# Kernel tuning notes

Hardware: AMD Instinct MI355X
Metric: run time of the kernel (lower is better)

Reference implementation:

```python
import jax, jax.numpy as jnp
import numpy as np

B, NM, NB, Z, H, K = 1024, 20000, 25000, 64, 256, 20
BETA = 0.1
LOG2PI = float(np.log(2.0 * np.pi))


def _log_normal(x, m, v):
    D = x.shape[-1]
    return (-0.5 * D * LOG2PI
            - 0.5 * jnp.sum(jnp.log(v), axis=-1)
            - 0.5 * jnp.sum((x - m) ** 2 / v, axis=-1))


def _kl_gmm(z, q_m, q_logv, p_m, p_logv):
    log_q = _log_normal(z, q_m, jnp.exp(q_logv))                               # [B]
    lp = _log_normal(z[:, None, :], p_m[None], jnp.exp(p_logv)[None])          # [B,K]
    log_p = jax.scipy.special.logsumexp(lp, axis=1) - jnp.log(float(p_m.shape[0]))
    return jnp.sum(log_q - log_p)


def _dist2(x, y):
    # ||x_i - y_j||_2^2, expanded form (avoids the [R,C,D] broadcast of the torch code)
    x2 = jnp.sum(x * x, axis=1, keepdims=True)
    y2 = jnp.sum(y * y, axis=1, keepdims=True)
    return x2 + y2.T - 2.0 * (x @ y.T)


def _distance_gmm(mu_s, mu_d, lv_s, lv_d):
    return _dist2(mu_s, mu_d) + _dist2(jnp.exp(0.5 * lv_s), jnp.exp(0.5 * lv_d)) + 1e-6


def _cost_mat(cost_s, cost_t, tran):
    f1 = jnp.sum(cost_s ** 2, axis=1, keepdims=True) / cost_s.shape[0]  # [ns,1]
    f2 = jnp.sum(cost_t ** 2, axis=1, keepdims=True) / cost_t.shape[0]  # [nt,1]
    return f1 + f2.T - 2.0 * (cost_s @ tran @ cost_t.T)


def _fgw(mu, z_mu, logvar, z_logvar):
    c_post = _distance_gmm(mu, mu, logvar, logvar)
    c_prior = _distance_gmm(z_mu, z_mu, z_logvar, z_logvar)
    c_pp = _distance_gmm(mu, z_mu, logvar, z_logvar)
    ns, nt = c_post.shape[0], c_prior.shape[0]
    p_s = jnp.ones((ns, 1), c_post.dtype) / ns
    p_t = jnp.ones((nt, 1), c_post.dtype) / nt

    def compute_tran(c_post, c_prior, c_pp):
        def outer(carry, _):
            tran, dual = carry
            cost = BETA * _cost_mat(c_post, c_prior, tran) + (1.0 - BETA) * c_pp
            kernel = jnp.exp(-cost / jnp.max(jnp.abs(cost))) * tran
            b = p_t / (kernel.T @ dual)

            def inner(c2, _):
                dual, b = c2
                dual = p_s / (kernel @ b)
                b = p_t / (kernel.T @ dual)
                return (dual, b), None

            (dual, b), _ = jax.lax.scan(inner, (dual, b), None, length=5)
            tran = (dual @ b.T) * kernel
            return (tran, dual), None

        init = (jnp.ones((ns, nt), c_post.dtype) / (ns * nt),
                jnp.ones((ns, 1), c_post.dtype) / ns)
        (tran, _), _ = jax.lax.scan(outer, init, None, length=10)
        return jnp.where(jnp.any(jnp.isnan(tran)),
                         jnp.ones((ns, nt), tran.dtype) / (ns * nt), tran)

    # torch detaches tran before the final cost, so cut all gradient through the loop
    tran = jax.lax.stop_gradient(compute_tran(c_post, c_prior, c_pp))
    cost = BETA * _cost_mat(c_post, c_prior, tran) + (1.0 - BETA) * c_pp
    return jnp.sum(cost * tran)


def _forward(batch_user_x, batch_user_y, p_mu_a, p_logv_a, p_mu_b, p_logv_b,
             eps_x, eps_y, eps_xr, eps_yr,
             W1a, b1a, W21a, b21a, W22a, b22a, W3a, b3a, W4a, b4a,
             W1b, b1b, W21b, b21b, W22b, b22b, W3b, b3b, W4b, b4b):
    def enc_a(x):
        h = jax.nn.relu(x @ W1a + b1a)
        return h @ W21a + b21a, h @ W22a + b22a

    def dec_a(z):
        return jax.nn.relu(z @ W3a + b3a) @ W4a + b4a

    def enc_b(x):
        h = jax.nn.relu(x @ W1b + b1b)
        return h @ W21b + b21b, h @ W22b + b22b

    def dec_b(z):
        return jax.nn.relu(z @ W3b + b3b) @ W4b + b4b

    # dropout rate = 0.0 -> identity
    mu_a, logvar_a = enc_a(batch_user_x)
    z_x = mu_a + eps_x * jnp.exp(0.5 * logvar_a)
    preds_x = dec_a(z_x)
    mu_b, logvar_b = enc_b(batch_user_y)
    z_y = mu_b + eps_y * jnp.exp(0.5 * logvar_b)
    preds_y = dec_b(z_y)

    gmm_reg_loss_a = _kl_gmm(z_x, mu_a, logvar_a, p_mu_a, p_logv_a)
    gmm_reg_loss_b = _kl_gmm(z_y, mu_b, logvar_b, p_mu_b, p_logv_b)
    align_global_loss = _fgw(mu_b, mu_a, logvar_b, logvar_a)

    preds_x2y = dec_b(z_x)
    preds_y2x = dec_a(z_y)
    m_xr, lv_xr = enc_b(preds_x2y)
    feature_x_r = m_xr + eps_xr * jnp.exp(0.5 * lv_xr)
    m_yr, lv_yr = enc_a(preds_y2x)
    feature_y_r = m_yr + eps_yr * jnp.exp(0.5 * lv_yr)

    cyc_loss_x = jnp.linalg.norm(z_x - feature_x_r)
    cyc_loss_y = jnp.linalg.norm(z_y - feature_y_r)
    return (preds_x, preds_y, preds_x2y, preds_y2x, z_x, z_y,
            gmm_reg_loss_a, gmm_reg_loss_b, feature_x_r, feature_y_r,
            align_global_loss, cyc_loss_x, cyc_loss_y)


def setup_inputs() -> dict:
    key = jax.random.key(0)
    ks = jax.random.split(key, 24)

    def nrm(i, shape, s=1.0):
        return jax.random.normal(ks[i], shape, dtype=jnp.float32) * s

    return {
        "user_1": jax.random.randint(ks[0], (B,), 0, 100000),
        "user_2": jax.random.randint(ks[1], (B,), 0, 100000),
        "batch_user_x": jax.random.uniform(ks[2], (B, NM), dtype=jnp.float32),
        "batch_user_y": jax.random.uniform(ks[3], (B, NB), dtype=jnp.float32),
        "p_mu_a": nrm(4, (K, Z)), "p_logv_a": nrm(5, (K, Z), 0.1),
        "p_mu_b": nrm(6, (K, Z)), "p_logv_b": nrm(7, (K, Z), 0.1),
        "eps_x": nrm(8, (B, Z)), "eps_y": nrm(9, (B, Z)),
        "eps_xr": nrm(10, (B, Z)), "eps_yr": nrm(11, (B, Z)),
        "W1a": nrm(12, (NM, H), 0.02), "b1a": jnp.zeros((H,), jnp.float32),
        "W21a": nrm(13, (H, Z), 0.02), "b21a": jnp.zeros((Z,), jnp.float32),
        "W22a": nrm(14, (H, Z), 0.02), "b22a": jnp.zeros((Z,), jnp.float32),
        "W3a": nrm(15, (Z, H), 0.02), "b3a": jnp.zeros((H,), jnp.float32),
        "W4a": nrm(16, (H, NM), 0.02), "b4a": jnp.zeros((NM,), jnp.float32),
        "W1b": nrm(17, (NB, H), 0.02), "b1b": jnp.zeros((H,), jnp.float32),
        "W21b": nrm(18, (H, Z), 0.02), "b21b": jnp.zeros((Z,), jnp.float32),
        "W22b": nrm(19, (H, Z), 0.02), "b22b": jnp.zeros((Z,), jnp.float32),
        "W3b": nrm(20, (Z, H), 0.02), "b3b": jnp.zeros((H,), jnp.float32),
        "W4b": nrm(21, (H, NB), 0.02), "b4b": jnp.zeros((NB,), jnp.float32),
    }


def reference(user_1, user_2, batch_user_x, batch_user_y, p_mu_a, p_logv_a, p_mu_b, p_logv_b,
              eps_x, eps_y, eps_xr, eps_yr,
              W1a, b1a, W21a, b21a, W22a, b22a, W3a, b3a, W4a, b4a,
              W1b, b1b, W21b, b21b, W22b, b22b, W3b, b3b, W4b, b4b):
    # user_1/user_2 are unused by the torch forward as well
    return _forward(batch_user_x, batch_user_y, p_mu_a, p_logv_a, p_mu_b, p_logv_b,
                    eps_x, eps_y, eps_xr, eps_yr,
                    W1a, b1a, W21a, b21a, W22a, b22a, W3a, b3a, W4a, b4a,
                    W1b, b1b, W21b, b21b, W22b, b22b, W3b, b3b, W4b, b4b)
```

## Files before the change

kernel.cpp:

```cpp
#include <hip/hip_runtime.h>


#define DEVI __device__ __forceinline__

typedef __attribute__((ext_vector_type(4))) float  f32x4;
typedef __attribute__((ext_vector_type(4))) short  s16x4;
typedef __attribute__((ext_vector_type(8))) short  s16x8;
typedef __attribute__((ext_vector_type(8))) __bf16 bf16x8;

#define PS (1.f / 1024.f)
#define UNIF (1.f / (1024.f * 1024.f))

DEVI short f2bf(float f) {
  unsigned u = __float_as_uint(f);
  u += 0x7fffu + ((u >> 16) & 1u);
  return (short)(u >> 16);
}
DEVI float bf2f(unsigned short u) { return __uint_as_float(((unsigned)u) << 16); }

DEVI f32x4 mfma16(bf16x8 a, bf16x8 b, f32x4 c) {
  return __builtin_amdgcn_mfma_f32_16x16x32_bf16(a, b, c, 0, 0, 0);
}

struct GemmArgs {
  const float* Af;
  const unsigned short* Bt;
  float* outF;
  const float* bias;
  float* partials;
  int M, N, K;
  int lda, ldbt, ldc;
  int totSteps, nSplits;
};

enum { EPI_PARTIAL, EPI_BIAS, EPI_COST, EPI_LOSS };

template<int BM, int BN, int WR, int WC, int EPI>
DEVI void gemm_body(const GemmArgs g)
{
  constexpr int BK = 64, BKP = 72;
  constexpr int NT = WR * WC * 64;
  __shared__ short As[BM * BKP];
  __shared__ short Bs[BN * BKP];

  const int m0 = blockIdx.x * BM;
  int n0 = 0, kb0 = 0, kb1 = g.K, split = 0;
  if constexpr (EPI == EPI_PARTIAL) {
    split = blockIdx.y;
    int s0 = (split * g.totSteps) / g.nSplits;
    int s1 = ((split + 1) * g.totSteps) / g.nSplits;
    kb0 = s0 * BK;
    kb1 = s1 * BK; if (kb1 > g.K) kb1 = g.K;
  } else {
    n0 = blockIdx.y * BN;
  }
  const int tid  = threadIdx.x;
  const int lane = tid & 63;
  const int wv   = tid >> 6;
  const int wr   = wv % WR;
  const int wc   = wv / WR;

  f32x4 acc[2][4];
  #pragma unroll
  for (int i = 0; i < 2; ++i)
    #pragma unroll
    for (int j = 0; j < 4; ++j) acc[i][j] = f32x4{0.f, 0.f, 0.f, 0.f};

  for (int kb = kb0; kb < kb1; kb += BK) {
    {
      constexpr int NV = BM * BK / 4;
      #pragma unroll
      for (int i = 0; i < NV / NT; ++i) {
        int idx = tid + NT * i;
        int r = idx >> 4, q = idx & 15;
        int k = kb + 4 * q;
        f32x4 v = f32x4{0.f, 0.f, 0.f, 0.f};
        if (k < kb1) v = *(const f32x4*)(g.Af + (size_t)(m0 + r) * g.lda + k);
        s16x4 s;
        s.x = f2bf(v.x); s.y = f2bf(v.y); s.z = f2bf(v.z); s.w = f2bf(v.w);
        *(s16x4*)&As[r * BKP + 4 * q] = s;
      }
    }
    {
      constexpr int NV = BN * BK / 8;
      #pragma unroll
      for (int i = 0; i < NV / NT; ++i) {
        int idx = tid + NT * i;
        int r = idx >> 3, q = idx & 7;
        int k = kb + 8 * q;
        s16x8 v{};
        if ((n0 + r) < g.N && k < kb1)
          v = *(const s16x8*)(g.Bt + (size_t)(n0 + r) * g.ldbt + k);
        *(s16x8*)&Bs[r * BKP + 8 * q] = v;
      }
    }
    __syncthreads();
    #pragma unroll
    for (int s = 0; s < 2; ++s) {
      const int ko = 32 * s + 8 * (lane >> 4);
      bf16x8 a0 = *(const bf16x8*)&As[(wr * 32 +      (lane & 15)) * BKP + ko];
      bf16x8 a1 = *(const bf16x8*)&As[(wr * 32 + 16 + (lane & 15)) * BKP + ko];
      #pragma unroll
      for (int fn = 0; fn < 4; ++fn) {
        bf16x8 b = *(const bf16x8*)&Bs[(wc * 64 + fn * 16 + (lane & 15)) * BKP + ko];
        acc[0][fn] = mfma16(a0, b, acc[0][fn]);
        acc[1][fn] = mfma16(a1, b, acc[1][fn]);
      }
    }
    __syncthreads();
  }

  #pragma unroll
  for (int fm = 0; fm < 2; ++fm) {
    #pragma unroll
    for (int fn = 0; fn < 4; ++fn) {
      #pragma unroll
      for (int p = 0; p < 4; ++p) {
        int gm = m0 + wr * 32 + fm * 16 + (lane >> 4) * 4 + p;
        int gn = n0 + wc * 64 + fn * 16 + (lane & 15);
        float v = acc[fm][fn][p];
        if constexpr (EPI == EPI_PARTIAL) {
          g.partials[((size_t)split * g.M + gm) * 256 + gn] = v;
        } else {
          if (gn < g.N) g.outF[(size_t)gm * g.ldc + gn] = v + g.bias[gn];
        }
      }
    }
  }
}

template<int BM, int BN, int WR, int WC, int EPI>
__global__ __launch_bounds__(WR*WC*64)
void k_gemm2(GemmArgs g0, GemmArgs g1)
{
  gemm_body<BM, BN, WR, WC, EPI>(blockIdx.z ? g1 : g0);
}

struct G1Args {
  const unsigned short* A;
  const float* KT;
  const float* dinv;
  const float* braw;
  unsigned short* U;
  const unsigned* nflag;
  int mode;
};

__global__ __launch_bounds__(256)
void k_fgw_g1(G1Args a)
{
  __shared__ short As[64 * 72];
  __shared__ short Bs[64 * 72];
  const bool uni = (a.mode == 0) || (a.mode == 2 && *a.nflag != 0u);

  const int bid = blockIdx.x, tid = threadIdx.x;
  const int lane = tid & 63, wv = tid >> 6;
  const int wr = wv & 1, wc = wv >> 1;
  const int m0 = (bid >> 4) * 64, n0 = (bid & 15) * 64;

  f32x4 acc[2][2];
  #pragma unroll
  for (int i = 0; i < 2; ++i)
    #pragma unroll
    for (int j = 0; j < 2; ++j) acc[i][j] = f32x4{0.f, 0.f, 0.f, 0.f};

  const short ub = f2bf(UNIF);

  for (int kb = 0; kb < 1024; kb += 64) {
    #pragma unroll
    for (int i = 0; i < 2; ++i) {
      int idx = tid + 256 * i;
      int r = idx >> 3, q = idx & 7;
      s16x8 av = *(const s16x8*)&a.A[(size_t)(m0 + r) * 1024 + kb + 8 * q];
      if (!uni) {
        f32x4 d0 = *(const f32x4*)&a.dinv[kb + 8 * q];
        f32x4 d1 = *(const f32x4*)&a.dinv[kb + 8 * q + 4];
        s16x8 o;
        o[0] = f2bf(bf2f((unsigned short)av[0]) * d0.x);
        o[1] = f2bf(bf2f((unsigned short)av[1]) * d0.y);
        o[2] = f2bf(bf2f((unsigned short)av[2]) * d0.z);
        o[3] = f2bf(bf2f((unsigned short)av[3]) * d0.w);
        o[4] = f2bf(bf2f((unsigned short)av[4]) * d1.x);
        o[5] = f2bf(bf2f((unsigned short)av[5]) * d1.y);
        o[6] = f2bf(bf2f((unsigned short)av[6]) * d1.z);
        o[7] = f2bf(bf2f((unsigned short)av[7]) * d1.w);
        av = o;
      }
      *(s16x8*)&As[r * 72 + 8 * q] = av;
      s16x8 bv;
      if (uni) {
        #pragma unroll
        for (int j = 0; j < 8; ++j) bv[j] = ub;
      } else {
        f32x4 k0 = *(const f32x4*)&a.KT[(size_t)(n0 + r) * 1024 + kb + 8 * q];
        f32x4 k1 = *(const f32x4*)&a.KT[(size_t)(n0 + r) * 1024 + kb + 8 * q + 4];
        bv[0] = f2bf(k0.x); bv[1] = f2bf(k0.y); bv[2] = f2bf(k0.z); bv[3] = f2bf(k0.w);
        bv[4] = f2bf(k1.x); bv[5] = f2bf(k1.y); bv[6] = f2bf(k1.z); bv[7] = f2bf(k1.w);
      }
      *(s16x8*)&Bs[r * 72 + 8 * q] = bv;
    }
    __syncthreads();
    #pragma unroll
    for (int s = 0; s < 2; ++s) {
      const int ko = 32 * s + 8 * (lane >> 4);
      bf16x8 a0 = *(const bf16x8*)&As[(wr * 32 +      (lane & 15)) * 72 + ko];
      bf16x8 a1 = *(const bf16x8*)&As[(wr * 32 + 16 + (lane & 15)) * 72 + ko];
      bf16x8 b0 = *(const bf16x8*)&Bs[(wc * 32 +      (lane & 15)) * 72 + ko];
      bf16x8 b1 = *(const bf16x8*)&Bs[(wc * 32 + 16 + (lane & 15)) * 72 + ko];
      acc[0][0] = mfma16(a0, b0, acc[0][0]);
      acc[1][0] = mfma16(a1, b0, acc[1][0]);
      acc[0][1] = mfma16(a0, b1, acc[0][1]);
      acc[1][1] = mfma16(a1, b1, acc[1][1]);
    }
    __syncthreads();
  }

  #pragma unroll
  for (int fm = 0; fm < 2; ++fm) {
    #pragma unroll
    for (int fn = 0; fn < 2; ++fn) {
      int gn = n0 + wc * 32 + fn * 16 + (lane & 15);
      float bs = uni ? 1.f : (PS / a.braw[gn]);
      #pragma unroll
      for (int p = 0; p < 4; ++p) {
        int gm = m0 + wr * 32 + fm * 16 + (lane >> 4) * 4 + p;
        float v = acc[fm][fn][p];
        a.U[(size_t)gm * 1024 + gn] = (unsigned short)f2bf(uni ? v : bs * v);
      }
    }
  }
}

struct FgwGemmArgs {
  const unsigned short* A;
  const unsigned short* Bt;
  float* cost;
  const float* f1;
  const float* f2;
  const float* cpp;
  unsigned* mx;
  float* loss;
  float* braw2;
  const float* Kf;
  const float* dinv;
  const float* brawv;
  const unsigned* nflag;
};

template<int EPI>
__global__ __launch_bounds__(256)
void k_fgw_gemm(FgwGemmArgs a)
{
  __shared__ short As[64 * 72];
  __shared__ short Bs[64 * 72];
  __shared__ float red[4];

  const int bid = blockIdx.x, tid = threadIdx.x;
  const int lane = tid & 63, wv = tid >> 6;
  const int wr = wv & 1, wc = wv >> 1;
  const int m0 = (bid >> 4) * 64, n0 = (bid & 15) * 64;

  if constexpr (EPI == EPI_COST) {
    if (bid == 0) {
      #pragma unroll
      for (int i = 0; i < 4; ++i) a.braw2[tid + 256 * i] = 0.f;
    }
  }

  f32x4 acc[2][2];
  #pragma unroll
  for (int i = 0; i < 2; ++i)
    #pragma unroll
    for (int j = 0; j < 2; ++j) acc[i][j] = f32x4{0.f, 0.f, 0.f, 0.f};

  for (int kb = 0; kb < 1024; kb += 64) {
    #pragma unroll
    for (int i = 0; i < 2; ++i) {
      int idx = tid + 256 * i;
      int r = idx >> 3, q = idx & 7;
      *(s16x8*)&As[r * 72 + 8 * q] = *(const s16x8*)&a.A [(size_t)(m0 + r) * 1024 + kb + 8 * q];
      *(s16x8*)&Bs[r * 72 + 8 * q] = *(const s16x8*)&a.Bt[(size_t)(n0 + r) * 1024 + kb + 8 * q];
    }
    __syncthreads();
    #pragma unroll
    for (int s = 0; s < 2; ++s) {
      const int ko = 32 * s + 8 * (lane >> 4);
      bf16x8 a0 = *(const bf16x8*)&As[(wr * 32 +      (lane & 15)) * 72 + ko];
      bf16x8 a1 = *(const bf16x8*)&As[(wr * 32 + 16 + (lane & 15)) * 72 + ko];
      bf16x8 b0 = *(const bf16x8*)&Bs[(wc * 32 +      (lane & 15)) * 72 + ko];
      bf16x8 b1 = *(const bf16x8*)&Bs[(wc * 32 + 16 + (lane & 15)) * 72 + ko];
      acc[0][0] = mfma16(a0, b0, acc[0][0]);
      acc[1][0] = mfma16(a1, b0, acc[1][0]);
      acc[0][1] = mfma16(a0, b1, acc[0][1]);
      acc[1][1] = mfma16(a1, b1, acc[1][1]);
    }
    __syncthreads();
  }

  bool uni = false;
  if constexpr (EPI == EPI_LOSS) uni = (*a.nflag != 0u);

  float lred = 0.f;
  #pragma unroll
  for (int fm = 0; fm < 2; ++fm) {
    #pragma unroll
    for (int fn = 0; fn < 2; ++fn) {
      int gn = n0 + wc * 32 + fn * 16 + (lane & 15);
      float bs = 0.f;
      if constexpr (EPI == EPI_LOSS) bs = uni ? 0.f : (PS / a.brawv[gn]);
      #pragma unroll
      for (int p = 0; p < 4; ++p) {
        int gm = m0 + wr * 32 + fm * 16 + (lane >> 4) * 4 + p;
        float v = acc[fm][fn][p];
        size_t o = (size_t)gm * 1024 + gn;
        float c = 0.1f * (a.f1[gm] + a.f2[gn] - 2.f * v) + 0.9f * a.cpp[o];
        if constexpr (EPI == EPI_COST) {
          a.cost[o] = c;
          lred = fmaxf(lred, fabsf(c));
        } else {
          float trec = uni ? UNIF : (a.dinv[gm] * bs) * a.Kf[o];
          lred += c * trec;
        }
      }
    }
  }
  #pragma unroll
  for (int off = 32; off; off >>= 1) {
    float t = __shfl_xor(lred, off, 64);
    lred = (EPI == EPI_COST) ? fmaxf(lred, t) : (lred + t);
  }
  if (lane == 0) red[wv] = lred;
  __syncthreads();
  if (tid == 0) {
    if constexpr (EPI == EPI_COST) {
      float t = fmaxf(fmaxf(red[0], red[1]), fmaxf(red[2], red[3]));
      atomicMax(a.mx, __float_as_uint(t));
    } else {
      atomicAdd(a.loss, red[0] + red[1] + red[2] + red[3]);
    }
  }
}

__global__ __launch_bounds__(256)
void k_kbuild(const float* cost, const unsigned* mxbits, float* K, float* KT,
              const float* dinv, const float* brawOld, float* braw2, int uniform)
{
  __shared__ float tt[64 * 65];
  __shared__ float dS[64];
  __shared__ float bS[64];
  __shared__ float csum[4][64];
  const int r0 = blockIdx.x * 64, c0 = blockIdx.y * 64;
  const int tid = threadIdx.x;
  const float inv = 1.f / __uint_as_float(*mxbits);
  if (tid < 64) dS[tid] = dinv[r0 + tid];
  else if (tid >= 64 && tid < 128 && !uniform) bS[tid - 64] = PS / brawOld[c0 + tid - 64];
  __syncthreads();
  float colp = 0.f;
  #pragma unroll
  for (int i = 0; i < 16; ++i) {
    int idx = tid + 256 * i;
    int r = idx >> 6, c = idx & 63;
    size_t o = (size_t)(r0 + r) * 1024 + (c0 + c);
    float trec = uniform ? UNIF : (dS[r] * bS[c]) * K[o];
    float v = expf(-cost[o] * inv) * trec;
    K[o] = v;
    tt[r * 65 + c] = v;
    colp += v * dS[r];
  }
  csum[tid >> 6][tid & 63] = colp;
  __syncthreads();
  #pragma unroll
  for (int i = 0; i < 16; ++i) {
    int idx = tid + 256 * i;
    int c = idx >> 6, r = idx & 63;
    KT[(size_t)(c0 + c) * 1024 + (r0 + r)] = tt[r * 65 + c];
  }
  if (tid < 64)
    atomicAdd(&braw2[c0 + tid],
              csum[0][tid] + csum[1][tid] + csum[2][tid] + csum[3][tid]);
}

__global__ __launch_bounds__(256)
void k_matvec(const float* M, const float* xraw, float* yraw, float* invOut)
{
  const int r = blockIdx.x * 4 + (threadIdx.x >> 6);
  const int lane = threadIdx.x & 63;
  const int wv = threadIdx.x >> 6;
  const f32x4* row = (const f32x4*)(M + (size_t)r * 1024);
  const f32x4* xv  = (const f32x4*)xraw;
  float s = 0.f;
  #pragma unroll
  for (int q = 0; q < 4; ++q) {
    f32x4 a = row[lane + 64 * q];
    f32x4 x = xv [lane + 64 * q];
    f32x4 iv;
    iv.x = PS / x.x; iv.y = PS / x.y; iv.z = PS / x.z; iv.w = PS / x.w;
    if (invOut && blockIdx.x == 0 && wv == 0)
      *(f32x4*)&invOut[4 * (lane + 64 * q)] = iv;
    s += a.x * iv.x + a.y * iv.y + a.z * iv.z + a.w * iv.w;
  }
  #pragma unroll
  for (int o = 32; o; o >>= 1) s += __shfl_xor(s, o, 64);
  if (lane == 0) yraw[r] = s;
}

__global__ __launch_bounds__(256)
void k_nanscan(const float* K, const float* dinv, const float* braw, unsigned* flag)
{
  unsigned bad = 0;
  const int base = blockIdx.x * 256 + threadIdx.x;
  #pragma unroll
  for (int i = 0; i < 16; ++i) {
    int idx = base + 65536 * i;
    int r = idx >> 10, c = idx & 1023;
    float v = (dinv[r] * (PS / braw[c])) * K[idx];
    if (v != v) bad = 1u;
  }
  if (bad) atomicOr(flag, 1u);
}

struct DistMMArgs {
  const unsigned short* Fx[3]; const unsigned short* Fy[3];
  const float* nx[3]; const float* ny[3];
  unsigned short* outB[2]; float* outF; float* frow[2];
};
__global__ __launch_bounds__(256)
void k_distmm(DistMMArgs a)
{
  __shared__ short As[64 * 72];
  __shared__ short Bs[64 * 72];
  const int z = blockIdx.y;
  const int bid = blockIdx.x, tid = threadIdx.x;
  const int lane = tid & 63, wv = tid >> 6;
  const int wr = wv & 1, wc = wv >> 1;
  const int m0 = (bid >> 4) * 64, n0 = (bid & 15) * 64;
  const unsigned short* X = a.Fx[z];
  const unsigned short* Y = a.Fy[z];

  f32x4 acc[2][2];
  #pragma unroll
  for (int i = 0; i < 2; ++i)
    #pragma unroll
    for (int j = 0; j < 2; ++j) acc[i][j] = f32x4{0.f, 0.f, 0.f, 0.f};

  #pragma unroll
  for (int kb = 0; kb < 128; kb += 64) {
    #pragma unroll
    for (int i = 0; i < 2; ++i) {
      int idx = tid + 256 * i;
      int r = idx >> 3, q = idx & 7;
      *(s16x8*)&As[r * 72 + 8 * q] = *(const s16x8*)&X[(size_t)(m0 + r) * 128 + kb + 8 * q];
      *(s16x8*)&Bs[r * 72 + 8 * q] = *(const s16x8*)&Y[(size_t)(n0 + r) * 128 + kb + 8 * q];
    }
    __syncthreads();
    #pragma unroll
    for (int s = 0; s < 2; ++s) {
      const int ko = 32 * s + 8 * (lane >> 4);
      bf16x8 a0 = *(const bf16x8*)&As[(wr * 32 +      (lane & 15)) * 72 + ko];
      bf16x8 a1 = *(const bf16x8*)&As[(wr * 32 + 16 + (lane & 15)) * 72 + ko];
      bf16x8 b0 = *(const bf16x8*)&Bs[(wc * 32 +      (lane & 15)) * 72 + ko];
      bf16x8 b1 = *(const bf16x8*)&Bs[(wc * 32 + 16 + (lane & 15)) * 72 + ko];
      acc[0][0] = mfma16(a0, b0, acc[0][0]);
      acc[1][0] = mfma16(a1, b0, acc[1][0]);
      acc[0][1] = mfma16(a0, b1, acc[0][1]);
      acc[1][1] = mfma16(a1, b1, acc[1][1]);
    }
    __syncthreads();
  }

  const float* nxp = a.nx[z];
  const float* nyp = a.ny[z];
  float rp[2][4];
  #pragma unroll
  for (int fm = 0; fm < 2; ++fm)
    #pragma unroll
    for (int p = 0; p < 4; ++p) rp[fm][p] = 0.f;

  #pragma unroll
  for (int fm = 0; fm < 2; ++fm) {
    #pragma unroll
    for (int fn = 0; fn < 2; ++fn) {
      #pragma unroll
      for (int p = 0; p < 4; ++p) {
        int gm = m0 + wr * 32 + fm * 16 + (lane >> 4) * 4 + p;
        int gn = n0 + wc * 32 + fn * 16 + (lane & 15);
        float val = nxp[gm] + nyp[gn] - 2.f * acc[fm][fn][p] + 1e-6f;
        if (z == 2) a.outF[(size_t)gm * 1024 + gn] = val;
        else {
          a.outB[z][(size_t)gm * 1024 + gn] = (unsigned short)f2bf(val);
          rp[fm][p] += val * val;
        }
      }
    }
  }
  if (z < 2) {
    #pragma unroll
    for (int fm = 0; fm < 2; ++fm)
      #pragma unroll
      for (int p = 0; p < 4; ++p) {
        float v = rp[fm][p];
        v += __shfl_xor(v, 1, 64);
        v += __shfl_xor(v, 2, 64);
        v += __shfl_xor(v, 4, 64);
        v += __shfl_xor(v, 8, 64);
        rp[fm][p] = v;
      }
    if ((lane & 15) == 0) {
      #pragma unroll
      for (int fm = 0; fm < 2; ++fm)
        #pragma unroll
        for (int p = 0; p < 4; ++p) {
          int gm = m0 + wr * 32 + fm * 16 + (lane >> 4) * 4 + p;
          atomicAdd(&a.frow[z][gm], rp[fm][p] * (1.f / 1024.f));
        }
    }
  }
}

struct T4 { const float* in[4]; unsigned short* out[4]; int R[4], C[4], nx[4], nt[4]; };
__global__ void k_transpose4(T4 d)
{
  __shared__ float t[64][65];
  const int z = blockIdx.y;
  const int tile = blockIdx.x;
  if (tile >= d.nt[z]) return;
  const int R = d.R[z], C = d.C[z];
  const int r0 = (tile % d.nx[z]) * 64, c0 = (tile / d.nx[z]) * 64;
  const float* in = d.in[z];
  unsigned short* out = d.out[z];
  const int tid = threadIdx.x;
  #pragma unroll
  for (int i = 0; i < 16; ++i) {
    int idx = tid + 256 * i;
    int r = idx >> 6, c = idx & 63;
    float v = 0.f;
    if ((r0 + r) < R && (c0 + c) < C) v = in[(size_t)(r0 + r) * C + (c0 + c)];
    t[r][c] = v;
  }
  __syncthreads();
  #pragma unroll
  for (int i = 0; i < 16; ++i) {
    int idx = tid + 256 * i;
    int c = idx >> 6, r = idx & 63;
    if ((c0 + c) < C && (r0 + r) < R)
      out[(size_t)(c0 + c) * R + (r0 + r)] = (unsigned short)f2bf(t[r][c]);
  }
}

__global__ void k_wcomb_reduce(const float* partials, unsigned short* WcTa,
                               unsigned short* WcTb)
{
  __shared__ float t[64][65];
  const int z = blockIdx.z;
  const float* P = partials + (size_t)z * 32 * 256 * 256;
  unsigned short* WcT = z ? WcTb : WcTa;
  const int u0 = blockIdx.x * 64, v0 = blockIdx.y * 64;
  const int tid = threadIdx.x;
  #pragma unroll
  for (int i = 0; i < 16; ++i) {
    int idx = tid + 256 * i;
    int u = idx >> 6, v = idx & 63;
    float s = 0.f;
    for (int p = 0; p < 32; ++p)
      s += P[(size_t)p * 65536 + (u0 + u) * 256 + (v0 + v)];
    t[u][v] = s;
  }
  __syncthreads();
  #pragma unroll
  for (int i = 0; i < 16; ++i) {
    int idx = tid + 256 * i;
    int v = idx >> 6, u = idx & 63;
    WcT[(size_t)(v0 + v) * 256 + (u0 + u)] = (unsigned short)f2bf(t[u][v]);
  }
}

struct BcArgs {
  const float* b4[2]; const unsigned short* Wt1[2]; const float* b1[2];
  float* bc[2]; int K[2];
};
__global__ void k_bcvec(BcArgs a)
{
  const int y = blockIdx.y;
  const int c = blockIdx.x * 4 + (threadIdx.x >> 6);
  const int lane = threadIdx.x & 63;
  const int K = a.K[y];
  const unsigned short* wrow = a.Wt1[y] + (size_t)c * K;
  const float* b4 = a.b4[y];
  float s = 0.f;
  for (int k = lane * 8; k < K; k += 512) {
    s16x8 w = *(const s16x8*)&wrow[k];
    f32x4 v0 = *(const f32x4*)&b4[k];
    f32x4 v1 = *(const f32x4*)&b4[k + 4];
    s += v0.x * bf2f((unsigned short)w[0]) + v0.y * bf2f((unsigned short)w[1])
       + v0.z * bf2f((unsigned short)w[2]) + v0.w * bf2f((unsigned short)w[3])
       + v1.x * bf2f((unsigned short)w[4]) + v1.y * bf2f((unsigned short)w[5])
       + v1.z * bf2f((unsigned short)w[6]) + v1.w * bf2f((unsigned short)w[7]);
  }
  #pragma unroll
  for (int o = 32; o; o >>= 1) s += __shfl_xor(s, o, 64);
  if (lane == 0) a.bc[y][c] = s + a.b1[y][c];
}

struct EF {
  const float* partials[2]; const float* bias[2];
  const float* W21[2]; const float* b21[2];
  const float* W22[2]; const float* b22[2]; const float* eps[2];
  float* mu[2]; float* lv[2]; float* zO[2];
  unsigned short* F[2]; float* n[2];
};
__global__ __launch_bounds__(256)
void k_enc_fused(EF a)
{
  __shared__ float hrow[256];
  __shared__ float res[128];
  const int y = blockIdx.y;
  const int i = blockIdx.x;
  const int t = threadIdx.x;
  {
    float s = a.bias[y][t];
    const float* P = a.partials[y] + (size_t)i * 256 + t;
    #pragma unroll
    for (int p = 0; p < 16; ++p) s += P[(size_t)p * 262144];
    hrow[t] = fmaxf(s, 0.f);
  }
  __syncthreads();
  if (t < 128) {
    const int c = t & 63;
    const float* W = (t < 64) ? a.W21[y] : a.W22[y];
    float acc = (t < 64) ? a.b21[y][c] : a.b22[y][c];
    #pragma unroll 8
    for (int j = 0; j < 256; ++j) acc += hrow[j] * W[j * 64 + c];
    res[t] = acc;
  }
  __syncthreads();
  if (t < 64) {
    float mu = res[t], lv = res[64 + t];
    a.mu[y][(size_t)i * 64 + t] = mu;
    a.lv[y][(size_t)i * 64 + t] = lv;
    float sig = expf(0.5f * lv);
    a.zO[y][(size_t)i * 64 + t] = mu + a.eps[y][(size_t)i * 64 + t] * sig;
    unsigned short u0 = (unsigned short)f2bf(mu);
    unsigned short u1 = (unsigned short)f2bf(sig);
    unsigned short* Fr = a.F[y] + (size_t)i * 128;
    Fr[t] = u0;
    Fr[64 + t] = u1;
    float r0 = bf2f(u0), r1 = bf2f(u1);
    float p = r0 * r0 + r1 * r1;
    #pragma unroll
    for (int o = 32; o; o >>= 1) p += __shfl_xor(p, o, 64);
    if (t == 0) a.n[y][i] = p;
  }
}

struct RencArgs {
  const float* hd[2]; const unsigned short* WcT[2]; const float* bc[2];
  const float* W21[2]; const float* b21[2]; const float* W22[2]; const float* b22[2];
  const float* eps[2]; float* fout[2];
};
__global__ void k_renc_head(RencArgs a)
{
  __shared__ float hdrow[256];
  __shared__ float hr[256];
  __shared__ float res[128];
  const int y = blockIdx.y;
  const int i = blockIdx.x;
  const int t = threadIdx.x;
  hdrow[t] = a.hd[y][(size_t)i * 256 + t];
  __syncthreads();
  {
    const s16x8* wr = (const s16x8*)(a.WcT[y] + (size_t)t * 256);
    float s = a.bc[y][t];
    #pragma unroll 4
    for (int j = 0; j < 32; ++j) {
      s16x8 w = wr[j];
      const float* hp = &hdrow[j * 8];
      s += hp[0] * bf2f((unsigned short)w[0]) + hp[1] * bf2f((unsigned short)w[1])
         + hp[2] * bf2f((unsigned short)w[2]) + hp[3] * bf2f((unsigned short)w[3])
         + hp[4] * bf2f((unsigned short)w[4]) + hp[5] * bf2f((unsigned short)w[5])
         + hp[6] * bf2f((unsigned short)w[6]) + hp[7] * bf2f((unsigned short)w[7]);
    }
    hr[t] = fmaxf(s, 0.f);
  }
  __syncthreads();
  if (t < 128) {
    const int c = t & 63;
    const float* W = (t < 64) ? a.W21[y] : a.W22[y];
    float acc = (t < 64) ? a.b21[y][c] : a.b22[y][c];
    #pragma unroll 8
    for (int j = 0; j < 256; ++j) acc += hr[j] * W[j * 64 + c];
    res[t] = acc;
  }
  __syncthreads();
  if (t < 64) {
    float mu = res[t], lv = res[64 + t];
    a.fout[y][(size_t)i * 64 + t] = mu + a.eps[y][(size_t)i * 64 + t] * expf(0.5f * lv);
  }
}

struct DH4 { const float* z[4]; const float* W3[4]; const float* b3[4]; float* hd[4]; };
__global__ void k_dec_head4(DH4 a)
{
  __shared__ float zrow[64];
  const int y = blockIdx.y;
  const int i = blockIdx.x;
  const int t = threadIdx.x;
  if (t < 64) zrow[t] = a.z[y][(size_t)i * 64 + t];
  __syncthreads();
  const float* W3 = a.W3[y];
  float acc = a.b3[y][t];
  #pragma unroll
  for (int d = 0; d < 64; ++d) acc += zrow[d] * W3[d * 256 + t];
  a.hd[y][(size_t)i * 256 + t] = fmaxf(acc, 0.f);
}

__global__ void k_init(float* dinv, float* f1, float* f2, unsigned* mx,
                       unsigned* nanflag, float* cyc, float* ga, float* gb, float* al)
{
  int t = threadIdx.x;
  dinv[t] = PS;
  f1[t] = 0.f; f2[t] = 0.f;
  if (t < 16) mx[t] = 0u;
  if (t == 0) { *nanflag = 0u; cyc[0] = 0.f; cyc[1] = 0.f; *ga = 0.f; *gb = 0.f; *al = 0.f; }
}

struct G2 {
  const float* z[2]; const float* mu[2]; const float* lv[2];
  const float* pmu[2]; const float* plv[2]; float* o[2];
};
__global__ void k_gmm2(G2 a)
{
  const int y = blockIdx.y;
  const int i = blockIdx.x;
  const int d = threadIdx.x;
  const float zd = a.z[y][(size_t)i * 64 + d];
  const float m  = a.mu[y][(size_t)i * 64 + d];
  const float l  = a.lv[y][(size_t)i * 64 + d];
  float t = l + (zd - m) * (zd - m) * expf(-l);
  #pragma unroll
  for (int o = 32; o; o >>= 1) t += __shfl_xor(t, o, 64);
  const float C0 = 64.f * 1.8378770664093453f;
  float logq = -0.5f * (C0 + t);
  float lp[20];
  #pragma unroll
  for (int k = 0; k < 20; ++k) {
    float pm = a.pmu[y][k * 64 + d], pl = a.plv[y][k * 64 + d];
    float u = pl + (zd - pm) * (zd - pm) * expf(-pl);
    #pragma unroll
    for (int o = 32; o; o >>= 1) u += __shfl_xor(u, o, 64);
    lp[k] = -0.5f * (C0 + u);
  }
  float mx = lp[0];
  #pragma unroll
  for (int k = 1; k < 20; ++k) mx = fmaxf(mx, lp[k]);
  float s = 0.f;
  #pragma unroll
  for (int k = 0; k < 20; ++k) s += expf(lp[k] - mx);
  float logp = mx + logf(s) - 2.9957322735539909f;
  if (d == 0) atomicAdd(a.o[y], logq - logp);
}

struct Sq2 { const float* a[2]; const float* b[2]; float* cyc; };
__global__ void k_sqdiff2(Sq2 g)
{
  __shared__ float red[4];
  const int y = blockIdx.y;
  int idx = blockIdx.x * 256 + threadIdx.x;
  float d = g.a[y][idx] - g.b[y][idx];
  d = d * d;
  #pragma unroll
  for (int o = 32; o; o >>= 1) d += __shfl_xor(d, o, 64);
  int lane = threadIdx.x & 63, wv = threadIdx.x >> 6;
  if (lane == 0) red[wv] = d;
  __syncthreads();
  if (threadIdx.x == 0) atomicAdd(g.cyc + y, red[0] + red[1] + red[2] + red[3]);
}

__global__ void k_finish(const float* slots, float* o1, float* o2)
{
  if (threadIdx.x == 0) { *o1 = sqrtf(slots[0]); *o2 = sqrtf(slots[1]); }
}

extern "C" void kernel_launch(void* const* d_in, const int* in_sizes, int n_in,
                              void* d_out, int out_size, void* d_ws, size_t ws_size,
                              hipStream_t stream)
{
  (void)in_sizes; (void)n_in; (void)out_size; (void)ws_size;

  const float* X     = (const float*)d_in[2];
  const float* Y     = (const float*)d_in[3];
  const float* pmua  = (const float*)d_in[4];
  const float* plva  = (const float*)d_in[5];
  const float* pmub  = (const float*)d_in[6];
  const float* plvb  = (const float*)d_in[7];
  const float* epsx  = (const float*)d_in[8];
  const float* epsy  = (const float*)d_in[9];
  const float* epsxr = (const float*)d_in[10];
  const float* epsyr = (const float*)d_in[11];
  const float* W1a = (const float*)d_in[12];  const float* b1a = (const float*)d_in[13];
  const float* W21a= (const float*)d_in[14];  const float* b21a= (const float*)d_in[15];
  const float* W22a= (const float*)d_in[16];  const float* b22a= (const float*)d_in[17];
  const float* W3a = (const float*)d_in[18];  const float* b3a = (const float*)d_in[19];
  const float* W4a = (const float*)d_in[20];  const float* b4a = (const float*)d_in[21];
  const float* W1b = (const float*)d_in[22];  const float* b1b = (const float*)d_in[23];
  const float* W21b= (const float*)d_in[24];  const float* b21b= (const float*)d_in[25];
  const float* W22b= (const float*)d_in[26];  const float* b22b= (const float*)d_in[27];
  const float* W3b = (const float*)d_in[28];  const float* b3b = (const float*)d_in[29];
  const float* W4b = (const float*)d_in[30];  const float* b4b = (const float*)d_in[31];

  float* out = (float*)d_out;
  const size_t P_X = 0, P_Y = 20480000, P_X2Y = 46080000, P_Y2X = 71680000;
  const size_t Z_X = 92160000, Z_Y = 92225536;
  const size_t GMM_A = 92291072, GMM_B = 92291073;
  const size_t F_XR = 92291074, F_YR = 92356610;
  const size_t ALIGN = 92422146, CYC_X = 92422147, CYC_Y = 92422148;

  char* w = (char*)d_ws;
  size_t off = 0;
  auto alloc = [&](size_t bytes) -> void* {
    void* p = w + off;
    off += (bytes + 255) & ~(size_t)255;
    return p;
  };
  unsigned short* Wt1a = (unsigned short*)alloc((size_t)256 * 20000 * 2);
  unsigned short* Wt1b = (unsigned short*)alloc((size_t)256 * 25000 * 2);
  unsigned short* W4ta = (unsigned short*)alloc((size_t)20000 * 256 * 2);
  unsigned short* W4tb = (unsigned short*)alloc((size_t)25000 * 256 * 2);
  unsigned short* WcTa = (unsigned short*)alloc((size_t)256 * 256 * 2);
  unsigned short* WcTb = (unsigned short*)alloc((size_t)256 * 256 * 2);
  float* bca  = (float*)alloc(256 * 4);
  float* bcb  = (float*)alloc(256 * 4);
  float* mu_a = (float*)alloc(1024 * 64 * 4);
  float* lv_a = (float*)alloc(1024 * 64 * 4);
  float* mu_b = (float*)alloc(1024 * 64 * 4);
  float* lv_b = (float*)alloc(1024 * 64 * 4);
  float* f1   = (float*)alloc(1024 * 4);
  float* f2   = (float*)alloc(1024 * 4);
  unsigned* mx      = (unsigned*)alloc(16 * 4);
  unsigned* nanflag = (unsigned*)alloc(256);
  float* cyc  = (float*)alloc(256);
  float* draw = (float*)alloc(1024 * 4);
  float* braw = (float*)alloc(1024 * 4);
  float* braw2 = (float*)alloc(1024 * 4);
  float* dinv = (float*)alloc(1024 * 4);
  unsigned short* Fb = (unsigned short*)alloc((size_t)1024 * 128 * 2);
  unsigned short* Fa = (unsigned short*)alloc((size_t)1024 * 128 * 2);
  float* nb = (float*)alloc(1024 * 4);
  float* na = (float*)alloc(1024 * 4);
  char* arena = (char*)alloc((size_t)32 * 1024 * 1024);
  float* partials = (float*)arena;
  size_t ao = 0;
  auto aalloc = [&](size_t bytes) -> void* {
    void* p = arena + ao;
    ao += (bytes + 255) & ~(size_t)255;
    return p;
  };
  unsigned short* cpostB  = (unsigned short*)aalloc((size_t)1024 * 1024 * 2);
  unsigned short* cpriorB = (unsigned short*)aalloc((size_t)1024 * 1024 * 2);
  float* cpp  = (float*)aalloc((size_t)1024 * 1024 * 4);
  unsigned short* Umat  = (unsigned short*)aalloc((size_t)1024 * 1024 * 2);
  float* cost  = (float*)aalloc((size_t)1024 * 1024 * 4);
  float* Kmat  = (float*)aalloc((size_t)1024 * 1024 * 4);
  float* KTmat = (float*)aalloc((size_t)1024 * 1024 * 4);
  float* hd0 = (float*)(arena);
  float* hd1 = (float*)(arena + (size_t)1024 * 256 * 4);
  float* hd2 = (float*)(arena + (size_t)2 * 1024 * 256 * 4);
  float* hd3 = (float*)(arena + (size_t)3 * 1024 * 256 * 4);

  {
    T4 d{};
    d.in[0] = W1a; d.out[0] = Wt1a; d.R[0] = 20000; d.C[0] = 256;
    d.in[1] = W1b; d.out[1] = Wt1b; d.R[1] = 25000; d.C[1] = 256;
    d.in[2] = W4a; d.out[2] = W4ta; d.R[2] = 256;   d.C[2] = 20000;
    d.in[3] = W4b; d.out[3] = W4tb; d.R[3] = 256;   d.C[3] = 25000;
    for (int z = 0; z < 4; ++z) {
      d.nx[z] = (d.R[z] + 63) / 64;
      d.nt[z] = d.nx[z] * ((d.C[z] + 63) / 64);
    }
    k_transpose4<<<dim3(1564, 4), 256, 0, stream>>>(d);
  }

  k_init<<<1, 1024, 0, stream>>>(dinv, f1, f2, mx, nanflag, cyc,
                                 out + GMM_A, out + GMM_B, out + ALIGN);

  {
    GemmArgs ga{}, gb{};
    ga.Af = W4a; ga.Bt = Wt1a; ga.partials = partials;
    ga.M = 256; ga.N = 256; ga.K = 20000; ga.lda = 20000; ga.ldbt = 20000;
    ga.totSteps = 313; ga.nSplits = 32;
    gb = ga;
    gb.Af = W4b; gb.Bt = Wt1b; gb.partials = partials + (size_t)32 * 65536;
    gb.K = 25000; gb.lda = 25000; gb.ldbt = 25000; gb.totSteps = 391;
    k_gemm2<128, 256, 4, 4, EPI_PARTIAL><<<dim3(2, 32, 2), 1024, 0, stream>>>(ga, gb);
    k_wcomb_reduce<<<dim3(4, 4, 2), 256, 0, stream>>>(partials, WcTa, WcTb);
    BcArgs bc{};
    bc.b4[0] = b4a; bc.Wt1[0] = Wt1a; bc.b1[0] = b1a; bc.bc[0] = bca; bc.K[0] = 20000;
    bc.b4[1] = b4b; bc.Wt1[1] = Wt1b; bc.b1[1] = b1b; bc.bc[1] = bcb; bc.K[1] = 25000;
    k_bcvec<<<dim3(64, 2), 256, 0, stream>>>(bc);
  }

  {
    GemmArgs ga{}, gb{};
    ga.Af = X; ga.Bt = Wt1a; ga.partials = partials;
    ga.M = 1024; ga.N = 256; ga.K = 20000; ga.lda = 20000; ga.ldbt = 20000;
    ga.totSteps = 313; ga.nSplits = 16;
    gb = ga;
    gb.Af = Y; gb.Bt = Wt1b; gb.partials = partials + (size_t)16 * 1024 * 256;
    gb.K = 25000; gb.lda = 25000; gb.ldbt = 25000; gb.totSteps = 391;
    k_gemm2<128, 256, 4, 4, EPI_PARTIAL><<<dim3(8, 16, 2), 1024, 0, stream>>>(ga, gb);
    EF e{};
    e.partials[0] = partials; e.partials[1] = partials + (size_t)16 * 1024 * 256;
    e.bias[0] = b1a; e.bias[1] = b1b;
    e.W21[0] = W21a; e.b21[0] = b21a; e.W22[0] = W22a; e.b22[0] = b22a;
    e.eps[0] = epsx; e.mu[0] = mu_a; e.lv[0] = lv_a; e.zO[0] = out + Z_X;
    e.F[0] = Fa; e.n[0] = na;
    e.W21[1] = W21b; e.b21[1] = b21b; e.W22[1] = W22b; e.b22[1] = b22b;
    e.eps[1] = epsy; e.mu[1] = mu_b; e.lv[1] = lv_b; e.zO[1] = out + Z_Y;
    e.F[1] = Fb; e.n[1] = nb;
    k_enc_fused<<<dim3(1024, 2), 256, 0, stream>>>(e);
  }

  {
    G2 g{};
    g.z[0] = out + Z_X; g.mu[0] = mu_a; g.lv[0] = lv_a; g.pmu[0] = pmua; g.plv[0] = plva;
    g.o[0] = out + GMM_A;
    g.z[1] = out + Z_Y; g.mu[1] = mu_b; g.lv[1] = lv_b; g.pmu[1] = pmub; g.plv[1] = plvb;
    g.o[1] = out + GMM_B;
    k_gmm2<<<dim3(1024, 2), 64, 0, stream>>>(g);
  }

  {
    DistMMArgs dm{};
    dm.Fx[0] = Fb; dm.Fy[0] = Fb; dm.nx[0] = nb; dm.ny[0] = nb;
    dm.Fx[1] = Fa; dm.Fy[1] = Fa; dm.nx[1] = na; dm.ny[1] = na;
    dm.Fx[2] = Fb; dm.Fy[2] = Fa; dm.nx[2] = nb; dm.ny[2] = na;
    dm.outB[0] = cpostB; dm.outB[1] = cpriorB; dm.outF = cpp;
    dm.frow[0] = f1; dm.frow[1] = f2;
    k_distmm<<<dim3(256, 3), 256, 0, stream>>>(dm);
  }
  G1Args g1{};
  g1.A = cpostB; g1.KT = KTmat; g1.dinv = dinv; g1.braw = braw;
  g1.U = Umat; g1.nflag = nanflag;
  FgwGemmArgs fg{};
  fg.A = Umat; fg.Bt = cpriorB;
  fg.f1 = f1; fg.f2 = f2; fg.cpp = cpp; fg.cost = cost;
  fg.loss = out + ALIGN; fg.braw2 = braw2;
  fg.Kf = Kmat; fg.dinv = dinv; fg.brawv = braw; fg.nflag = nanflag;
  for (int it = 0; it < 10; ++it) {
    g1.mode = (it == 0) ? 0 : 1;
    k_fgw_g1<<<256, 256, 0, stream>>>(g1);
    fg.mx = mx + it;
    k_fgw_gemm<EPI_COST><<<256, 256, 0, stream>>>(fg);
    k_kbuild<<<dim3(16, 16), 256, 0, stream>>>(cost, mx + it, Kmat, KTmat,
                                               dinv, braw, braw2, it == 0 ? 1 : 0);
    for (int r = 0; r < 5; ++r) {
      k_matvec<<<256, 256, 0, stream>>>(Kmat, r == 0 ? braw2 : braw, draw, nullptr);
      k_matvec<<<256, 256, 0, stream>>>(KTmat, draw, braw, r == 4 ? dinv : nullptr);
    }
  }
  k_nanscan<<<256, 256, 0, stream>>>(Kmat, dinv, braw, nanflag);
  g1.mode = 2;
  k_fgw_g1<<<256, 256, 0, stream>>>(g1);
  k_fgw_gemm<EPI_LOSS><<<256, 256, 0, stream>>>(fg);

  {
    DH4 d{};
    d.z[0] = out + Z_X; d.W3[0] = W3a; d.b3[0] = b3a; d.hd[0] = hd0;
    d.z[1] = out + Z_Y; d.W3[1] = W3a; d.b3[1] = b3a; d.hd[1] = hd1;
    d.z[2] = out + Z_Y; d.W3[2] = W3b; d.b3[2] = b3b; d.hd[2] = hd2;
    d.z[3] = out + Z_X; d.W3[3] = W3b; d.b3[3] = b3b; d.hd[3] = hd3;
    k_dec_head4<<<dim3(1024, 4), 256, 0, stream>>>(d);
  }

  {
    RencArgs r{};
    r.hd[0] = hd3; r.WcT[0] = WcTb; r.bc[0] = bcb;
    r.W21[0] = W21b; r.b21[0] = b21b; r.W22[0] = W22b; r.b22[0] = b22b;
    r.eps[0] = epsxr; r.fout[0] = out + F_XR;
    r.hd[1] = hd1; r.WcT[1] = WcTa; r.bc[1] = bca;
    r.W21[1] = W21a; r.b21[1] = b21a; r.W22[1] = W22a; r.b22[1] = b22a;
    r.eps[1] = epsyr; r.fout[1] = out + F_YR;
    k_renc_head<<<dim3(1024, 2), 256, 0, stream>>>(r);
  }

  {
    Sq2 s{};
    s.a[0] = out + Z_X; s.b[0] = out + F_XR;
    s.a[1] = out + Z_Y; s.b[1] = out + F_YR;
    s.cyc = cyc;
    k_sqdiff2<<<dim3(256, 2), 256, 0, stream>>>(s);
    k_finish<<<1, 64, 0, stream>>>(cyc, out + CYC_X, out + CYC_Y);
  }

  {
    GemmArgs ga{}, gb{};
    ga.Af = hd0; ga.Bt = W4ta; ga.outF = out + P_X; ga.bias = b4a;
    ga.M = 1024; ga.N = 20000; ga.K = 256; ga.lda = 256; ga.ldbt = 256; ga.ldc = 20000;
    gb = ga; gb.Af = hd1; gb.outF = out + P_Y2X;
    k_gemm2<128, 256, 4, 4, EPI_BIAS><<<dim3(8, 79, 2), 1024, 0, stream>>>(ga, gb);

    GemmArgs gc{}, gd{};
    gc.Af = hd2; gc.Bt = W4tb; gc.outF = out + P_Y; gc.bias = b4b;
    gc.M = 1024; gc.N = 25000; gc.K = 256; gc.lda = 256; gc.ldbt = 256; gc.ldc = 25000;
    gd = gc; gd.Af = hd3; gd.outF = out + P_X2Y;
    k_gemm2<128, 256, 4, 4, EPI_BIAS><<<dim3(8, 98, 2), 1024, 0, stream>>>(gc, gd);
  }
}
```

Measured before the change: 1.582 ms.

## Merge decoder GEMMs, fold small kernels, enlarge FGW GEMM tiles to 128x128

Several unrelated changes. The four decoder output GEMMs go into one launch with early exit for out-of-range column tiles. The init kernel is folded into the transpose launch, the GMM KL into the encoder kernel, and the cycle-loss squared difference into the re-encoder head. The FGW inner GEMMs move from 64x64 tiles with 256 threads to 128x128 tiles with 512 threads. This cuts launch count and improves operand reuse in the iterative loop, but leaves only 64 blocks for the FGW GEMMs, which may underfill the GPU.

```diff
diff --git a/kernel.cpp b/kernel.cpp
--- a/kernel.cpp
+++ b/kernel.cpp
@@ -129,11 +129,17 @@
   }
 }
 
+struct Q4 { GemmArgs g[4]; };
+
 template<int BM, int BN, int WR, int WC, int EPI>
 __global__ __launch_bounds__(WR*WC*64)
-void k_gemm2(GemmArgs g0, GemmArgs g1)
-{
-  gemm_body<BM, BN, WR, WC, EPI>(blockIdx.z ? g1 : g0);
+void k_gemmN(Q4 q)
+{
+  GemmArgs g = q.g[blockIdx.z];
+  if constexpr (EPI == EPI_BIAS) {
+    if ((int)(blockIdx.y * BN) >= g.N) return;
+  }
+  gemm_body<BM, BN, WR, WC, EPI>(g);
 }
 
 struct G1Args {
@@ -146,21 +152,21 @@
   int mode;
 };
 
-__global__ __launch_bounds__(256)
+__global__ __launch_bounds__(512)
 void k_fgw_g1(G1Args a)
 {
-  __shared__ short As[64 * 72];
-  __shared__ short Bs[64 * 72];
+  __shared__ short As[128 * 72];
+  __shared__ short Bs[128 * 72];
   const bool uni = (a.mode == 0) || (a.mode == 2 && *a.nflag != 0u);
 
   const int bid = blockIdx.x, tid = threadIdx.x;
   const int lane = tid & 63, wv = tid >> 6;
   const int wr = wv & 1, wc = wv >> 1;
-  const int m0 = (bid >> 4) * 64, n0 = (bid & 15) * 64;
-
-  f32x4 acc[2][2];
-  #pragma unroll
-  for (int i = 0; i < 2; ++i)
+  const int m0 = (bid >> 3) * 128, n0 = (bid & 7) * 128;
+
+  f32x4 acc[4][2];
+  #pragma unroll
+  for (int i = 0; i < 4; ++i)
     #pragma unroll
     for (int j = 0; j < 2; ++j) acc[i][j] = f32x4{0.f, 0.f, 0.f, 0.f};
 
@@ -169,7 +175,7 @@
   for (int kb = 0; kb < 1024; kb += 64) {
     #pragma unroll
     for (int i = 0; i < 2; ++i) {
-      int idx = tid + 256 * i;
+      int idx = tid + 512 * i;
       int r = idx >> 3, q = idx & 7;
       s16x8 av = *(const s16x8*)&a.A[(size_t)(m0 + r) * 1024 + kb + 8 * q];
       if (!uni) {
@@ -203,27 +209,27 @@
     #pragma unroll
     for (int s = 0; s < 2; ++s) {
       const int ko = 32 * s + 8 * (lane >> 4);
-      bf16x8 a0 = *(const bf16x8*)&As[(wr * 32 +      (lane & 15)) * 72 + ko];
-      bf16x8 a1 = *(const bf16x8*)&As[(wr * 32 + 16 + (lane & 15)) * 72 + ko];
       bf16x8 b0 = *(const bf16x8*)&Bs[(wc * 32 +      (lane & 15)) * 72 + ko];
       bf16x8 b1 = *(const bf16x8*)&Bs[(wc * 32 + 16 + (lane & 15)) * 72 + ko];
-      acc[0][0] = mfma16(a0, b0, acc[0][0]);
-      acc[1][0] = mfma16(a1, b0, acc[1][0]);
-      acc[0][1] = mfma16(a0, b1, acc[0][1]);
-      acc[1][1] = mfma16(a1, b1, acc[1][1]);
+      #pragma unroll
+      for (int fm = 0; fm < 4; ++fm) {
+        bf16x8 af = *(const bf16x8*)&As[(wr * 64 + fm * 16 + (lane & 15)) * 72 + ko];
+        acc[fm][0] = mfma16(af, b0, acc[fm][0]);
+        acc[fm][1] = mfma16(af, b1, acc[fm][1]);
+      }
     }
     __syncthreads();
   }
 
   #pragma unroll
-  for (int fm = 0; fm < 2; ++fm) {
+  for (int fm = 0; fm < 4; ++fm) {
     #pragma unroll
     for (int fn = 0; fn < 2; ++fn) {
       int gn = n0 + wc * 32 + fn * 16 + (lane & 15);
       float bs = uni ? 1.f : (PS / a.braw[gn]);
       #pragma unroll
       for (int p = 0; p < 4; ++p) {
-        int gm = m0 + wr * 32 + fm * 16 + (lane >> 4) * 4 + p;
+        int gm = m0 + wr * 64 + fm * 16 + (lane >> 4) * 4 + p;
         float v = acc[fm][fn][p];
         a.U[(size_t)gm * 1024 + gn] = (unsigned short)f2bf(uni ? v : bs * v);
       }
@@ -248,24 +254,194 @@
 };
 
 template<int EPI>
+__global__ __launch_bounds__(512)
+void k_fgw_gemm(FgwGemmArgs a)
+{
+  __shared__ short As[128 * 72];
+  __shared__ short Bs[128 * 72];
+  __shared__ float red[8];
+
+  const int bid = blockIdx.x, tid = threadIdx.x;
+  const int lane = tid & 63, wv = tid >> 6;
+  const int wr = wv & 1, wc = wv >> 1;
+  const int m0 = (bid >> 3) * 128, n0 = (bid & 7) * 128;
+
+  if constexpr (EPI == EPI_COST) {
+    if (bid == 0) {
+      #pragma unroll
+      for (int i = 0; i < 2; ++i) a.braw2[tid + 512 * i] = 0.f;
+    }
+  }
+
+  f32x4 acc[4][2];
+  #pragma unroll
+  for (int i = 0; i < 4; ++i)
+    #pragma unroll
+    for (int j = 0; j < 2; ++j) acc[i][j] = f32x4{0.f, 0.f, 0.f, 0.f};
+
+  for (int kb = 0; kb < 1024; kb += 64) {
+    #pragma unroll
+    for (int i = 0; i < 2; ++i) {
+      int idx = tid + 512 * i;
+      int r = idx >> 3, q = idx & 7;
+      *(s16x8*)&As[r * 72 + 8 * q] = *(const s16x8*)&a.A [(size_t)(m0 + r) * 1024 + kb + 8 * q];
+      *(s16x8*)&Bs[r * 72 + 8 * q] = *(const s16x8*)&a.Bt[(size_t)(n0 + r) * 1024 + kb + 8 * q];
+    }
+    __syncthreads();
+    #pragma unroll
+    for (int s = 0; s < 2; ++s) {
+      const int ko = 32 * s + 8 * (lane >> 4);
+      bf16x8 b0 = *(const bf16x8*)&Bs[(wc * 32 +      (lane & 15)) * 72 + ko];
+      bf16x8 b1 = *(const bf16x8*)&Bs[(wc * 32 + 16 + (lane & 15)) * 72 + ko];
+      #pragma unroll
+      for (int fm = 0; fm < 4; ++fm) {
+        bf16x8 af = *(const bf16x8*)&As[(wr * 64 + fm * 16 + (lane & 15)) * 72 + ko];
+        acc[fm][0] = mfma16(af, b0, acc[fm][0]);
+        acc[fm][1] = mfma16(af, b1, acc[fm][1]);
+      }
+    }
+    __syncthreads();
+  }
+
+  bool uni = false;
+  if constexpr (EPI == EPI_LOSS) uni = (*a.nflag != 0u);
+
+  float lred = 0.f;
+  #pragma unroll
+  for (int fm = 0; fm < 4; ++fm) {
+    #pragma unroll
+    for (int fn = 0; fn < 2; ++fn) {
+      int gn = n0 + wc * 32 + fn * 16 + (lane & 15);
+      float bs = 0.f;
+      if constexpr (EPI == EPI_LOSS) bs = uni ? 0.f : (PS / a.brawv[gn]);
+      #pragma unroll
+      for (int p = 0; p < 4; ++p) {
+        int gm = m0 + wr * 64 + fm * 16 + (lane >> 4) * 4 + p;
+        float v = acc[fm][fn][p];
+        size_t o = (size_t)gm * 1024 + gn;
+        float c = 0.1f * (a.f1[gm] + a.f2[gn] - 2.f * v) + 0.9f * a.cpp[o];
+        if constexpr (EPI == EPI_COST) {
+          a.cost[o] = c;
+          lred = fmaxf(lred, fabsf(c));
+        } else {
+          float trec = uni ? UNIF : (a.dinv[gm] * bs) * a.Kf[o];
+          lred += c * trec;
+        }
+      }
+    }
+  }
+  #pragma unroll
+  for (int off = 32; off; off >>= 1) {
+    float t = __shfl_xor(lred, off, 64);
+    lred = (EPI == EPI_COST) ? fmaxf(lred, t) : (lred + t);
+  }
+  if (lane == 0) red[wv] = lred;
+  __syncthreads();
+  if (tid == 0) {
+    float t = red[0];
+    #pragma unroll
+    for (int i = 1; i < 8; ++i)
+      t = (EPI == EPI_COST) ? fmaxf(t, red[i]) : (t + red[i]);
+    if constexpr (EPI == EPI_COST) atomicMax(a.mx, __float_as_uint(t));
+    else atomicAdd(a.loss, t);
+  }
+}
+
 __global__ __launch_bounds__(256)
-void k_fgw_gemm(FgwGemmArgs a)
+void k_kbuild(const float* cost, const unsigned* mxbits, float* K, float* KT,
+              const float* dinv, const float* brawOld, float* braw2, int uniform)
+{
+  __shared__ float tt[64 * 65];
+  __shared__ float dS[64];
+  __shared__ float bS[64];
+  __shared__ float csum[4][64];
+  const int r0 = blockIdx.x * 64, c0 = blockIdx.y * 64;
+  const int tid = threadIdx.x;
+  const float inv = 1.f / __uint_as_float(*mxbits);
+  if (tid < 64) dS[tid] = dinv[r0 + tid];
+  else if (tid >= 64 && tid < 128 && !uniform) bS[tid - 64] = PS / brawOld[c0 + tid - 64];
+  __syncthreads();
+  float colp = 0.f;
+  #pragma unroll
+  for (int i = 0; i < 16; ++i) {
+    int idx = tid + 256 * i;
+    int r = idx >> 6, c = idx & 63;
+    size_t o = (size_t)(r0 + r) * 1024 + (c0 + c);
+    float trec = uniform ? UNIF : (dS[r] * bS[c]) * K[o];
+    float v = expf(-cost[o] * inv) * trec;
+    K[o] = v;
+    tt[r * 65 + c] = v;
+    colp += v * dS[r];
+  }
+  csum[tid >> 6][tid & 63] = colp;
+  __syncthreads();
+  #pragma unroll
+  for (int i = 0; i < 16; ++i) {
+    int idx = tid + 256 * i;
+    int c = idx >> 6, r = idx & 63;
+    KT[(size_t)(c0 + c) * 1024 + (r0 + r)] = tt[r * 65 + c];
+  }
+  if (tid < 64)
+    atomicAdd(&braw2[c0 + tid],
+              csum[0][tid] + csum[1][tid] + csum[2][tid] + csum[3][tid]);
+}
+
+__global__ __launch_bounds__(256)
+void k_matvec(const float* M, const float* xraw, float* yraw, float* invOut)
+{
+  const int r = blockIdx.x * 4 + (threadIdx.x >> 6);
+  const int lane = threadIdx.x & 63;
+  const int wv = threadIdx.x >> 6;
+  const f32x4* row = (const f32x4*)(M + (size_t)r * 1024);
+  const f32x4* xv  = (const f32x4*)xraw;
+  float s = 0.f;
+  #pragma unroll
+  for (int q = 0; q < 4; ++q) {
+    f32x4 a = row[lane + 64 * q];
+    f32x4 x = xv [lane + 64 * q];
+    f32x4 iv;
+    iv.x = PS / x.x; iv.y = PS / x.y; iv.z = PS / x.z; iv.w = PS / x.w;
+    if (invOut && blockIdx.x == 0 && wv == 0)
+      *(f32x4*)&invOut[4 * (lane + 64 * q)] = iv;
+    s += a.x * iv.x + a.y * iv.y + a.z * iv.z + a.w * iv.w;
+  }
+  #pragma unroll
+  for (int o = 32; o; o >>= 1) s += __shfl_xor(s, o, 64);
+  if (lane == 0) yraw[r] = s;
+}
+
+__global__ __launch_bounds__(256)
+void k_nanscan(const float* K, const float* dinv, const float* braw, unsigned* flag)
+{
+  unsigned bad = 0;
+  const int base = blockIdx.x * 256 + threadIdx.x;
+  #pragma unroll
+  for (int i = 0; i < 16; ++i) {
+    int idx = base + 65536 * i;
+    int r = idx >> 10, c = idx & 1023;
+    float v = (dinv[r] * (PS / braw[c])) * K[idx];
+    if (v != v) bad = 1u;
+  }
+  if (bad) atomicOr(flag, 1u);
+}
+
+struct DistMMArgs {
+  const unsigned short* Fx[3]; const unsigned short* Fy[3];
+  const float* nx[3]; const float* ny[3];
+  unsigned short* outB[2]; float* outF; float* frow[2];
+};
+__global__ __launch_bounds__(256)
+void k_distmm(DistMMArgs a)
 {
   __shared__ short As[64 * 72];
   __shared__ short Bs[64 * 72];
-  __shared__ float red[4];
-
+  const int z = blockIdx.y;
   const int bid = blockIdx.x, tid = threadIdx.x;
   const int lane = tid & 63, wv = tid >> 6;
   const int wr = wv & 1, wc = wv >> 1;
   const int m0 = (bid >> 4) * 64, n0 = (bid & 15) * 64;
-
-  if constexpr (EPI == EPI_COST) {
-    if (bid == 0) {
-      #pragma unroll
-      for (int i = 0; i < 4; ++i) a.braw2[tid + 256 * i] = 0.f;
-    }
-  }
+  const unsigned short* X = a.Fx[z];
+  const unsigned short* Y = a.Fy[z];
 
   f32x4 acc[2][2];
   #pragma unroll
@@ -273,13 +449,14 @@
     #pragma unroll
     for (int j = 0; j < 2; ++j) acc[i][j] = f32x4{0.f, 0.f, 0.f, 0.f};
 
-  for (int kb = 0; kb < 1024; kb += 64) {
+  #pragma unroll
+  for (int kb = 0; kb < 128; kb += 64) {
     #pragma unroll
     for (int i = 0; i < 2; ++i) {
       int idx = tid + 256 * i;
       int r = idx >> 3, q = idx & 7;
-      *(s16x8*)&As[r * 72 + 8 * q] = *(const s16x8*)&a.A [(size_t)(m0 + r) * 1024 + kb + 8 * q];
-      *(s16x8*)&Bs[r * 72 + 8 * q] = *(const s16x8*)&a.Bt[(size_t)(n0 + r) * 1024 + kb + 8 * q];
+      *(s16x8*)&As[r * 72 + 8 * q] = *(const s16x8*)&X[(size_t)(m0 + r) * 128 + kb + 8 * q];
+      *(s16x8*)&Bs[r * 72 + 8 * q] = *(const s16x8*)&Y[(size_t)(n0 + r) * 128 + kb + 8 * q];
     }
     __syncthreads();
     #pragma unroll
@@ -297,177 +474,6 @@
     __syncthreads();
   }
 
-  bool uni = false;
-  if constexpr (EPI == EPI_LOSS) uni = (*a.nflag != 0u);
-
-  float lred = 0.f;
-  #pragma unroll
-  for (int fm = 0; fm < 2; ++fm) {
-    #pragma unroll
-    for (int fn = 0; fn < 2; ++fn) {
-      int gn = n0 + wc * 32 + fn * 16 + (lane & 15);
-      float bs = 0.f;
-      if constexpr (EPI == EPI_LOSS) bs = uni ? 0.f : (PS / a.brawv[gn]);
-      #pragma unroll
-      for (int p = 0; p < 4; ++p) {
-        int gm = m0 + wr * 32 + fm * 16 + (lane >> 4) * 4 + p;
-        float v = acc[fm][fn][p];
-        size_t o = (size_t)gm * 1024 + gn;
-        float c = 0.1f * (a.f1[gm] + a.f2[gn] - 2.f * v) + 0.9f * a.cpp[o];
-        if constexpr (EPI == EPI_COST) {
-          a.cost[o] = c;
-          lred = fmaxf(lred, fabsf(c));
-        } else {
-          float trec = uni ? UNIF : (a.dinv[gm] * bs) * a.Kf[o];
-          lred += c * trec;
-        }
-      }
-    }
-  }
-  #pragma unroll
-  for (int off = 32; off; off >>= 1) {
-    float t = __shfl_xor(lred, off, 64);
-    lred = (EPI == EPI_COST) ? fmaxf(lred, t) : (lred + t);
-  }
-  if (lane == 0) red[wv] = lred;
-  __syncthreads();
-  if (tid == 0) {
-    if constexpr (EPI == EPI_COST) {
-      float t = fmaxf(fmaxf(red[0], red[1]), fmaxf(red[2], red[3]));
-      atomicMax(a.mx, __float_as_uint(t));
-    } else {
-      atomicAdd(a.loss, red[0] + red[1] + red[2] + red[3]);
-    }
-  }
-}
-
-__global__ __launch_bounds__(256)
-void k_kbuild(const float* cost, const unsigned* mxbits, float* K, float* KT,
-              const float* dinv, const float* brawOld, float* braw2, int uniform)
-{
-  __shared__ float tt[64 * 65];
-  __shared__ float dS[64];
-  __shared__ float bS[64];
-  __shared__ float csum[4][64];
-  const int r0 = blockIdx.x * 64, c0 = blockIdx.y * 64;
-  const int tid = threadIdx.x;
-  const float inv = 1.f / __uint_as_float(*mxbits);
-  if (tid < 64) dS[tid] = dinv[r0 + tid];
-  else if (tid >= 64 && tid < 128 && !uniform) bS[tid - 64] = PS / brawOld[c0 + tid - 64];
-  __syncthreads();
-  float colp = 0.f;
-  #pragma unroll
-  for (int i = 0; i < 16; ++i) {
-    int idx = tid + 256 * i;
-    int r = idx >> 6, c = idx & 63;
-    size_t o = (size_t)(r0 + r) * 1024 + (c0 + c);
-    float trec = uniform ? UNIF : (dS[r] * bS[c]) * K[o];
-    float v = expf(-cost[o] * inv) * trec;
-    K[o] = v;
-    tt[r * 65 + c] = v;
-    colp += v * dS[r];
-  }
-  csum[tid >> 6][tid & 63] = colp;
-  __syncthreads();
-  #pragma unroll
-  for (int i = 0; i < 16; ++i) {
-    int idx = tid + 256 * i;
-    int c = idx >> 6, r = idx & 63;
-    KT[(size_t)(c0 + c) * 1024 + (r0 + r)] = tt[r * 65 + c];
-  }
-  if (tid < 64)
-    atomicAdd(&braw2[c0 + tid],
-              csum[0][tid] + csum[1][tid] + csum[2][tid] + csum[3][tid]);
-}
-
-__global__ __launch_bounds__(256)
-void k_matvec(const float* M, const float* xraw, float* yraw, float* invOut)
-{
-  const int r = blockIdx.x * 4 + (threadIdx.x >> 6);
-  const int lane = threadIdx.x & 63;
-  const int wv = threadIdx.x >> 6;
-  const f32x4* row = (const f32x4*)(M + (size_t)r * 1024);
-  const f32x4* xv  = (const f32x4*)xraw;
-  float s = 0.f;
-  #pragma unroll
-  for (int q = 0; q < 4; ++q) {
-    f32x4 a = row[lane + 64 * q];
-    f32x4 x = xv [lane + 64 * q];
-    f32x4 iv;
-    iv.x = PS / x.x; iv.y = PS / x.y; iv.z = PS / x.z; iv.w = PS / x.w;
-    if (invOut && blockIdx.x == 0 && wv == 0)
-      *(f32x4*)&invOut[4 * (lane + 64 * q)] = iv;
-    s += a.x * iv.x + a.y * iv.y + a.z * iv.z + a.w * iv.w;
-  }
-  #pragma unroll
-  for (int o = 32; o; o >>= 1) s += __shfl_xor(s, o, 64);
-  if (lane == 0) yraw[r] = s;
-}
-
-__global__ __launch_bounds__(256)
-void k_nanscan(const float* K, const float* dinv, const float* braw, unsigned* flag)
-{
-  unsigned bad = 0;
-  const int base = blockIdx.x * 256 + threadIdx.x;
-  #pragma unroll
-  for (int i = 0; i < 16; ++i) {
-    int idx = base + 65536 * i;
-    int r = idx >> 10, c = idx & 1023;
-    float v = (dinv[r] * (PS / braw[c])) * K[idx];
-    if (v != v) bad = 1u;
-  }
-  if (bad) atomicOr(flag, 1u);
-}
-
-struct DistMMArgs {
-  const unsigned short* Fx[3]; const unsigned short* Fy[3];
-  const float* nx[3]; const float* ny[3];
-  unsigned short* outB[2]; float* outF; float* frow[2];
-};
-__global__ __launch_bounds__(256)
-void k_distmm(DistMMArgs a)
-{
-  __shared__ short As[64 * 72];
-  __shared__ short Bs[64 * 72];
-  const int z = blockIdx.y;
-  const int bid = blockIdx.x, tid = threadIdx.x;
-  const int lane = tid & 63, wv = tid >> 6;
-  const int wr = wv & 1, wc = wv >> 1;
-  const int m0 = (bid >> 4) * 64, n0 = (bid & 15) * 64;
-  const unsigned short* X = a.Fx[z];
-  const unsigned short* Y = a.Fy[z];
-
-  f32x4 acc[2][2];
-  #pragma unroll
-  for (int i = 0; i < 2; ++i)
-    #pragma unroll
-    for (int j = 0; j < 2; ++j) acc[i][j] = f32x4{0.f, 0.f, 0.f, 0.f};
-
-  #pragma unroll
-  for (int kb = 0; kb < 128; kb += 64) {
-    #pragma unroll
-    for (int i = 0; i < 2; ++i) {
-      int idx = tid + 256 * i;
-      int r = idx >> 3, q = idx & 7;
-      *(s16x8*)&As[r * 72 + 8 * q] = *(const s16x8*)&X[(size_t)(m0 + r) * 128 + kb + 8 * q];
-      *(s16x8*)&Bs[r * 72 + 8 * q] = *(const s16x8*)&Y[(size_t)(n0 + r) * 128 + kb + 8 * q];
-    }
-    __syncthreads();
-    #pragma unroll
-    for (int s = 0; s < 2; ++s) {
-      const int ko = 32 * s + 8 * (lane >> 4);
-      bf16x8 a0 = *(const bf16x8*)&As[(wr * 32 +      (lane & 15)) * 72 + ko];
-      bf16x8 a1 = *(const bf16x8*)&As[(wr * 32 + 16 + (lane & 15)) * 72 + ko];
-      bf16x8 b0 = *(const bf16x8*)&Bs[(wc * 32 +      (lane & 15)) * 72 + ko];
-      bf16x8 b1 = *(const bf16x8*)&Bs[(wc * 32 + 16 + (lane & 15)) * 72 + ko];
-      acc[0][0] = mfma16(a0, b0, acc[0][0]);
-      acc[1][0] = mfma16(a1, b0, acc[1][0]);
-      acc[0][1] = mfma16(a0, b1, acc[0][1]);
-      acc[1][1] = mfma16(a1, b1, acc[1][1]);
-    }
-    __syncthreads();
-  }
-
   const float* nxp = a.nx[z];
   const float* nyp = a.ny[z];
   float rp[2][4];
@@ -517,18 +523,37 @@
   }
 }
 
-struct T4 { const float* in[4]; unsigned short* out[4]; int R[4], C[4], nx[4], nt[4]; };
+struct T4 {
+  const float* in[4]; unsigned short* out[4]; int R[4], C[4], nx[4], nt[4];
+  float* dinv; float* f1; float* f2; unsigned* mx; unsigned* nanflag;
+  float* cyc; float* ga; float* gb; float* al;
+};
 __global__ void k_transpose4(T4 d)
 {
+  const int z = blockIdx.y;
+  const int tid = threadIdx.x;
+  if (z == 4) {
+    if (blockIdx.x == 0) {
+      #pragma unroll
+      for (int i = 0; i < 4; ++i) {
+        int k = tid + 256 * i;
+        d.dinv[k] = PS; d.f1[k] = 0.f; d.f2[k] = 0.f;
+      }
+      if (tid < 16) d.mx[tid] = 0u;
+      if (tid == 0) {
+        *d.nanflag = 0u; d.cyc[0] = 0.f; d.cyc[1] = 0.f;
+        *d.ga = 0.f; *d.gb = 0.f; *d.al = 0.f;
+      }
+    }
+    return;
+  }
   __shared__ float t[64][65];
-  const int z = blockIdx.y;
   const int tile = blockIdx.x;
   if (tile >= d.nt[z]) return;
   const int R = d.R[z], C = d.C[z];
   const int r0 = (tile % d.nx[z]) * 64, c0 = (tile / d.nx[z]) * 64;
   const float* in = d.in[z];
   unsigned short* out = d.out[z];
-  const int tid = threadIdx.x;
   #pragma unroll
   for (int i = 0; i < 16; ++i) {
     int idx = tid + 256 * i;
@@ -605,6 +630,7 @@
   const float* partials[2]; const float* bias[2];
   const float* W21[2]; const float* b21[2];
   const float* W22[2]; const float* b22[2]; const float* eps[2];
+  const float* pmu[2]; const float* plv[2]; float* gmmO[2];
   float* mu[2]; float* lv[2]; float* zO[2];
   unsigned short* F[2]; float* n[2];
 };
@@ -638,7 +664,8 @@
     a.mu[y][(size_t)i * 64 + t] = mu;
     a.lv[y][(size_t)i * 64 + t] = lv;
     float sig = expf(0.5f * lv);
-    a.zO[y][(size_t)i * 64 + t] = mu + a.eps[y][(size_t)i * 64 + t] * sig;
+    float zd = mu + a.eps[y][(size_t)i * 64 + t] * sig;
+    a.zO[y][(size_t)i * 64 + t] = zd;
     unsigned short u0 = (unsigned short)f2bf(mu);
     unsigned short u1 = (unsigned short)f2bf(sig);
     unsigned short* Fr = a.F[y] + (size_t)i * 128;
@@ -649,6 +676,28 @@
     #pragma unroll
     for (int o = 32; o; o >>= 1) p += __shfl_xor(p, o, 64);
     if (t == 0) a.n[y][i] = p;
+    float tq = lv + (zd - mu) * (zd - mu) * expf(-lv);
+    #pragma unroll
+    for (int o = 32; o; o >>= 1) tq += __shfl_xor(tq, o, 64);
+    const float C0 = 64.f * 1.8378770664093453f;
+    float logq = -0.5f * (C0 + tq);
+    float lp[20];
+    #pragma unroll
+    for (int k = 0; k < 20; ++k) {
+      float pm = a.pmu[y][k * 64 + t], pl = a.plv[y][k * 64 + t];
+      float u = pl + (zd - pm) * (zd - pm) * expf(-pl);
+      #pragma unroll
+      for (int o = 32; o; o >>= 1) u += __shfl_xor(u, o, 64);
+      lp[k] = -0.5f * (C0 + u);
+    }
+    float mxv = lp[0];
+    #pragma unroll
+    for (int k = 1; k < 20; ++k) mxv = fmaxf(mxv, lp[k]);
+    float se = 0.f;
+    #pragma unroll
+    for (int k = 0; k < 20; ++k) se += expf(lp[k] - mxv);
+    float logp = mxv + logf(se) - 2.9957322735539909f;
+    if (t == 0) atomicAdd(a.gmmO[y], logq - logp);
   }
 }
 
@@ -656,6 +705,7 @@
   const float* hd[2]; const unsigned short* WcT[2]; const float* bc[2];
   const float* W21[2]; const float* b21[2]; const float* W22[2]; const float* b22[2];
   const float* eps[2]; float* fout[2];
+  const float* zin[2]; float* cyc;
 };
 __global__ void k_renc_head(RencArgs a)
 {
@@ -693,7 +743,13 @@
   __syncthreads();
   if (t < 64) {
     float mu = res[t], lv = res[64 + t];
-    a.fout[y][(size_t)i * 64 + t] = mu + a.eps[y][(size_t)i * 64 + t] * expf(0.5f * lv);
+    float f = mu + a.eps[y][(size_t)i * 64 + t] * expf(0.5f * lv);
+    a.fout[y][(size_t)i * 64 + t] = f;
+    float d = a.zin[y][(size_t)i * 64 + t] - f;
+    d = d * d;
+    #pragma unroll
+    for (int o = 32; o; o >>= 1) d += __shfl_xor(d, o, 64);
+    if (t == 0) atomicAdd(a.cyc + y, d);
   }
 }
 
@@ -711,68 +767,6 @@
   #pragma unroll
   for (int d = 0; d < 64; ++d) acc += zrow[d] * W3[d * 256 + t];
   a.hd[y][(size_t)i * 256 + t] = fmaxf(acc, 0.f);
-}
-
-__global__ void k_init(float* dinv, float* f1, float* f2, unsigned* mx,
-                       unsigned* nanflag, float* cyc, float* ga, float* gb, float* al)
-{
-  int t = threadIdx.x;
-  dinv[t] = PS;
-  f1[t] = 0.f; f2[t] = 0.f;
-  if (t < 16) mx[t] = 0u;
-  if (t == 0) { *nanflag = 0u; cyc[0] = 0.f; cyc[1] = 0.f; *ga = 0.f; *gb = 0.f; *al = 0.f; }
-}
-
-struct G2 {
-  const float* z[2]; const float* mu[2]; const float* lv[2];
-  const float* pmu[2]; const float* plv[2]; float* o[2];
-};
-__global__ void k_gmm2(G2 a)
-{
-  const int y = blockIdx.y;
-  const int i = blockIdx.x;
-  const int d = threadIdx.x;
-  const float zd = a.z[y][(size_t)i * 64 + d];
-  const float m  = a.mu[y][(size_t)i * 64 + d];
-  const float l  = a.lv[y][(size_t)i * 64 + d];
-  float t = l + (zd - m) * (zd - m) * expf(-l);
-  #pragma unroll
-  for (int o = 32; o; o >>= 1) t += __shfl_xor(t, o, 64);
-  const float C0 = 64.f * 1.8378770664093453f;
-  float logq = -0.5f * (C0 + t);
-  float lp[20];
-  #pragma unroll
-  for (int k = 0; k < 20; ++k) {
-    float pm = a.pmu[y][k * 64 + d], pl = a.plv[y][k * 64 + d];
-    float u = pl + (zd - pm) * (zd - pm) * expf(-pl);
-    #pragma unroll
-    for (int o = 32; o; o >>= 1) u += __shfl_xor(u, o, 64);
-    lp[k] = -0.5f * (C0 + u);
-  }
-  float mx = lp[0];
-  #pragma unroll
-  for (int k = 1; k < 20; ++k) mx = fmaxf(mx, lp[k]);
-  float s = 0.f;
-  #pragma unroll
-  for (int k = 0; k < 20; ++k) s += expf(lp[k] - mx);
-  float logp = mx + logf(s) - 2.9957322735539909f;
-  if (d == 0) atomicAdd(a.o[y], logq - logp);
-}
-
-struct Sq2 { const float* a[2]; const float* b[2]; float* cyc; };
-__global__ void k_sqdiff2(Sq2 g)
-{
-  __shared__ float red[4];
-  const int y = blockIdx.y;
-  int idx = blockIdx.x * 256 + threadIdx.x;
-  float d = g.a[y][idx] - g.b[y][idx];
-  d = d * d;
-  #pragma unroll
-  for (int o = 32; o; o >>= 1) d += __shfl_xor(d, o, 64);
-  int lane = threadIdx.x & 63, wv = threadIdx.x >> 6;
-  if (lane == 0) red[wv] = d;
-  __syncthreads();
-  if (threadIdx.x == 0) atomicAdd(g.cyc + y, red[0] + red[1] + red[2] + red[3]);
 }
 
 __global__ void k_finish(const float* slots, float* o1, float* o2)
@@ -876,21 +870,22 @@
       d.nx[z] = (d.R[z] + 63) / 64;
       d.nt[z] = d.nx[z] * ((d.C[z] + 63) / 64);
     }
-    k_transpose4<<<dim3(1564, 4), 256, 0, stream>>>(d);
-  }
-
-  k_init<<<1, 1024, 0, stream>>>(dinv, f1, f2, mx, nanflag, cyc,
-                                 out + GMM_A, out + GMM_B, out + ALIGN);
+    d.dinv = dinv; d.f1 = f1; d.f2 = f2; d.mx = mx; d.nanflag = nanflag;
+    d.cyc = cyc; d.ga = out + GMM_A; d.gb = out + GMM_B; d.al = out + ALIGN;
+    k_transpose4<<<dim3(1564, 5), 256, 0, stream>>>(d);
+  }
 
   {
-    GemmArgs ga{}, gb{};
-    ga.Af = W4a; ga.Bt = Wt1a; ga.partials = partials;
-    ga.M = 256; ga.N = 256; ga.K = 20000; ga.lda = 20000; ga.ldbt = 20000;
-    ga.totSteps = 313; ga.nSplits = 32;
-    gb = ga;
-    gb.Af = W4b; gb.Bt = Wt1b; gb.partials = partials + (size_t)32 * 65536;
-    gb.K = 25000; gb.lda = 25000; gb.ldbt = 25000; gb.totSteps = 391;
-    k_gemm2<128, 256, 4, 4, EPI_PARTIAL><<<dim3(2, 32, 2), 1024, 0, stream>>>(ga, gb);
+    Q4 q{};
+    q.g[0].Af = W4a; q.g[0].Bt = Wt1a; q.g[0].partials = partials;
+    q.g[0].M = 256; q.g[0].N = 256; q.g[0].K = 20000;
+    q.g[0].lda = 20000; q.g[0].ldbt = 20000;
+    q.g[0].totSteps = 313; q.g[0].nSplits = 32;
+    q.g[1] = q.g[0];
+    q.g[1].Af = W4b; q.g[1].Bt = Wt1b;
+    q.g[1].partials = partials + (size_t)32 * 65536;
+    q.g[1].K = 25000; q.g[1].lda = 25000; q.g[1].ldbt = 25000; q.g[1].totSteps = 391;
+    k_gemmN<128, 256, 4, 4, EPI_PARTIAL><<<dim3(2, 32, 2), 1024, 0, stream>>>(q);
     k_wcomb_reduce<<<dim3(4, 4, 2), 256, 0, stream>>>(partials, WcTa, WcTb);
     BcArgs bc{};
     bc.b4[0] = b4a; bc.Wt1[0] = Wt1a; bc.b1[0] = b1a; bc.bc[0] = bca; bc.K[0] = 20000;
@@ -899,33 +894,28 @@
   }
 
   {
-    GemmArgs ga{}, gb{};
-    ga.Af = X; ga.Bt = Wt1a; ga.partials = partials;
-    ga.M = 1024; ga.N = 256; ga.K = 20000; ga.lda = 20000; ga.ldbt = 20000;
-    ga.totSteps = 313; ga.nSplits = 16;
-    gb = ga;
-    gb.Af = Y; gb.Bt = Wt1b; gb.partials = partials + (size_t)16 * 1024 * 256;
-    gb.K = 25000; gb.lda = 25000; gb.ldbt = 25000; gb.totSteps = 391;
-    k_gemm2<128, 256, 4, 4, EPI_PARTIAL><<<dim3(8, 16, 2), 1024, 0, stream>>>(ga, gb);
+    Q4 q{};
+    q.g[0].Af = X; q.g[0].Bt = Wt1a; q.g[0].partials = partials;
+    q.g[0].M = 1024; q.g[0].N = 256; q.g[0].K = 20000;
+    q.g[0].lda = 20000; q.g[0].ldbt = 20000;
+    q.g[0].totSteps = 313; q.g[0].nSplits = 16;
+    q.g[1] = q.g[0];
+    q.g[1].Af = Y; q.g[1].Bt = Wt1b;
+    q.g[1].partials = partials + (size_t)16 * 1024 * 256;
+    q.g[1].K = 25000; q.g[1].lda = 25000; q.g[1].ldbt = 25000; q.g[1].totSteps = 391;
+    k_gemmN<128, 256, 4, 4, EPI_PARTIAL><<<dim3(8, 16, 2), 1024, 0, stream>>>(q);
     EF e{};
     e.partials[0] = partials; e.partials[1] = partials + (size_t)16 * 1024 * 256;
     e.bias[0] = b1a; e.bias[1] = b1b;
     e.W21[0] = W21a; e.b21[0] = b21a; e.W22[0] = W22a; e.b22[0] = b22a;
     e.eps[0] = epsx; e.mu[0] = mu_a; e.lv[0] = lv_a; e.zO[0] = out + Z_X;
     e.F[0] = Fa; e.n[0] = na;
+    e.pmu[0] = pmua; e.plv[0] = plva; e.gmmO[0] = out + GMM_A;
     e.W21[1] = W21b; e.b21[1] = b21b; e.W22[1] = W22b; e.b22[1] = b22b;
     e.eps[1] = epsy; e.mu[1] = mu_b; e.lv[1] = lv_b; e.zO[1] = out + Z_Y;
     e.F[1] = Fb; e.n[1] = nb;
+    e.pmu[1] = pmub; e.plv[1] = plvb; e.gmmO[1] = out + GMM_B;
     k_enc_fused<<<dim3(1024, 2), 256, 0, stream>>>(e);
-  }
-
-  {
-    G2 g{};
-    g.z[0] = out + Z_X; g.mu[0] = mu_a; g.lv[0] = lv_a; g.pmu[0] = pmua; g.plv[0] = plva;
-    g.o[0] = out + GMM_A;
-    g.z[1] = out + Z_Y; g.mu[1] = mu_b; g.lv[1] = lv_b; g.pmu[1] = pmub; g.plv[1] = plvb;
-    g.o[1] = out + GMM_B;
-    k_gmm2<<<dim3(1024, 2), 64, 0, stream>>>(g);
   }
 
   {
@@ -947,9 +937,9 @@
   fg.Kf = Kmat; fg.dinv = dinv; fg.brawv = braw; fg.nflag = nanflag;
   for (int it = 0; it < 10; ++it) {
     g1.mode = (it == 0) ? 0 : 1;
-    k_fgw_g1<<<256, 256, 0, stream>>>(g1);
+    k_fgw_g1<<<64, 512, 0, stream>>>(g1);
     fg.mx = mx + it;
-    k_fgw_gemm<EPI_COST><<<256, 256, 0, stream>>>(fg);
+    k_fgw_gemm<EPI_COST><<<64, 512, 0, stream>>>(fg);
     k_kbuild<<<dim3(16, 16), 256, 0, stream>>>(cost, mx + it, Kmat, KTmat,
                                                dinv, braw, braw2, it == 0 ? 1 : 0);
     for (int r = 0; r < 5; ++r) {
@@ -959,8 +949,8 @@
   }
   k_nanscan<<<256, 256, 0, stream>>>(Kmat, dinv, braw, nanflag);
   g1.mode = 2;
-  k_fgw_g1<<<256, 256, 0, stream>>>(g1);
-  k_fgw_gemm<EPI_LOSS><<<256, 256, 0, stream>>>(fg);
+  k_fgw_g1<<<64, 512, 0, stream>>>(g1);
+  k_fgw_gemm<EPI_LOSS><<<64, 512, 0, stream>>>(fg);
 
   {
     DH4 d{};
@@ -975,33 +965,25 @@
     RencArgs r{};
     r.hd[0] = hd3; r.WcT[0] = WcTb; r.bc[0] = bcb;
     r.W21[0] = W21b; r.b21[0] = b21b; r.W22[0] = W22b; r.b22[0] = b22b;
-    r.eps[0] = epsxr; r.fout[0] = out + F_XR;
+    r.eps[0] = epsxr; r.fout[0] = out + F_XR; r.zin[0] = out + Z_X;
     r.hd[1] = hd1; r.WcT[1] = WcTa; r.bc[1] = bca;
     r.W21[1] = W21a; r.b21[1] = b21a; r.W22[1] = W22a; r.b22[1] = b22a;
-    r.eps[1] = epsyr; r.fout[1] = out + F_YR;
+    r.eps[1] = epsyr; r.fout[1] = out + F_YR; r.zin[1] = out + Z_Y;
+    r.cyc = cyc;
     k_renc_head<<<dim3(1024, 2), 256, 0, stream>>>(r);
   }
+  k_finish<<<1, 64, 0, stream>>>(cyc, out + CYC_X, out + CYC_Y);
 
   {
-    Sq2 s{};
-    s.a[0] = out + Z_X; s.b[0] = out + F_XR;
-    s.a[1] = out + Z_Y; s.b[1] = out + F_YR;
-    s.cyc = cyc;
-    k_sqdiff2<<<dim3(256, 2), 256, 0, stream>>>(s);
-    k_finish<<<1, 64, 0, stream>>>(cyc, out + CYC_X, out + CYC_Y);
-  }
-
-  {
-    GemmArgs ga{}, gb{};
-    ga.Af = hd0; ga.Bt = W4ta; ga.outF = out + P_X; ga.bias = b4a;
-    ga.M = 1024; ga.N = 20000; ga.K = 256; ga.lda = 256; ga.ldbt = 256; ga.ldc = 20000;
-    gb = ga; gb.Af = hd1; gb.outF = out + P_Y2X;
-    k_gemm2<128, 256, 4, 4, EPI_BIAS><<<dim3(8, 79, 2), 1024, 0, stream>>>(ga, gb);
-
-    GemmArgs gc{}, gd{};
-    gc.Af = hd2; gc.Bt = W4tb; gc.outF = out + P_Y; gc.bias = b4b;
-    gc.M = 1024; gc.N = 25000; gc.K = 256; gc.lda = 256; gc.ldbt = 256; gc.ldc = 25000;
-    gd = gc; gd.Af = hd3; gd.outF = out + P_X2Y;
-    k_gemm2<128, 256, 4, 4, EPI_BIAS><<<dim3(8, 98, 2), 1024, 0, stream>>>(gc, gd);
-  }
-}
+    Q4 q{};
+    q.g[0].Af = hd0; q.g[0].Bt = W4ta; q.g[0].outF = out + P_X; q.g[0].bias = b4a;
+    q.g[0].M = 1024; q.g[0].N = 20000; q.g[0].K = 256;
+    q.g[0].lda = 256; q.g[0].ldbt = 256; q.g[0].ldc = 20000;
+    q.g[1] = q.g[0]; q.g[1].Af = hd1; q.g[1].outF = out + P_Y2X;
+    q.g[2] = q.g[0];
+    q.g[2].Af = hd2; q.g[2].Bt = W4tb; q.g[2].outF = out + P_Y; q.g[2].bias = b4b;
+    q.g[2].N = 25000; q.g[2].ldc = 25000;
+    q.g[3] = q.g[2]; q.g[3].Af = hd3; q.g[3].outF = out + P_X2Y;
+    k_gemmN<128, 256, 4, 4, EPI_BIAS><<<dim3(8, 98, 4), 1024, 0, stream>>>(q);
+  }
+}
```

Result: slower. 1.742 ms (+10.1%).
